# Kernel optimization log

Measured on AMD Instinct MI355X. Metric: run time of the kernel, lower is better.

## Reference

```python
import jax, jax.numpy as jnp
import numpy as np

# dims forced by module structure (see shape_source)
DA, DV, DD, NL, L, R0 = 128, 96, 64, 8, 2, 1.0
ATOMS, EDGES, BATCH = 5000, 40000, 1


def radial_encode_8(rvec, r0):
    # reconstruction: 8 Gaussian RBFs on |r|/r0 with centers k/7
    r = jnp.sqrt(jnp.sum(rvec * rvec, axis=-1) + 1e-12)
    u = r / r0
    k = jnp.arange(NL, dtype=u.dtype)
    return jnp.exp(-0.5 * (u[..., None] * 7.0 - k) ** 2)  # (E, 8)


def tens_sigmoid(x):
    # equivariant sigmoid: rescale vector by bounded function of its norm
    n = jnp.sqrt(jnp.sum(x * x, axis=-1, keepdims=True) + 1e-12)
    return x * (2.0 * jax.nn.sigmoid(n) - 1.0) / n


def _forward(src, dst, r_ij, x_a, x_v, x_d,
             P_000, P_110, P_220, P_011, P_101, P_121, P_211, P_111,
             P_022, P_202, P_112, P_222, P_212,
             W_in_a, W_in_v, W_in_d, W_out_a, W_out_v, W_out_d,
             Wd_a, W1_a, b1_a, W2_a, b2_a, W3_a, b3_a,
             Vd_v, V1_v, V2_v, V3_v):
    b, A = x_a.shape[:2]
    # read-in, then fuse L into the batch dim (high-actv layout)
    a = jnp.einsum('oc,bnc->bno', W_in_a, x_a).reshape(b, A, L, DA).transpose(2, 0, 1, 3).reshape(L * b, A, DA)
    v = jnp.einsum('oc,bnci->bnoi', W_in_v, x_v).reshape(b, A, L, DV, 3).transpose(2, 0, 1, 3, 4).reshape(L * b, A, DV, 3)
    d = jnp.einsum('oc,bncij->bnoij', W_in_d, x_d).reshape(b, A, L, DD, 3, 3).transpose(2, 0, 1, 3, 4, 5).reshape(L * b, A, DD, 3, 3)

    rad = radial_encode_8(r_ij, R0)              # (E, 8)
    rh = tens_sigmoid(r_ij * (7.0 / R0))         # (E, 3)
    pa = rad                                      # (E, 8)
    pv = rad[:, :, None] * rh[:, None, :]         # (E, 8, 3)
    pd = rad[:, :, None, None] * rh[:, None, None, :] * rh[:, None, :, None]  # (E, 8, 3, 3)

    # edge gather (dst nodes)
    aj, vj, dj = a[:, dst], v[:, dst], d[:, dst]

    # Ant16: 13 fused equivariant tensor-product contractions
    psi_a = (jnp.einsum('alc,el,bec->bea', P_000, pa, aj)
             + jnp.einsum('alc,eli,beci->bea', P_110, pv, vj)
             + jnp.einsum('alc,elij,becij->bea', P_220, pd, dj))

    def cross1(P, phi, xv):
        t = lambda j, k: jnp.einsum('vlc,el,bec->bev', P, phi[:, :, j], xv[:, :, :, k])
        return jnp.stack([t(1, 2) - t(2, 1), t(2, 0) - t(0, 2), t(0, 1) - t(1, 0)], axis=-1)

    psi_v = (jnp.einsum('vlc,el,beci->bevi', P_011, pa, vj)
             + jnp.einsum('vlc,eli,bec->bevi', P_101, pv, aj)
             + jnp.einsum('vlc,elj,becij->bevi', P_121, pv, dj)
             + jnp.einsum('vlc,elij,becj->bevi', P_211, pd, vj)
             + cross1(P_111, pv, vj))

    def cross2(P, phid, xv):
        t = lambda k, m: jnp.einsum('dlc,elj,bec->bedj', P, phid[:, :, k, :], xv[:, :, :, m])
        return jnp.stack([t(1, 2) - t(2, 1), t(2, 0) - t(0, 2), t(0, 1) - t(1, 0)], axis=-2)

    psi_d = (jnp.einsum('dlc,el,becij->bedij', P_022, pa, dj)
             + jnp.einsum('dlc,elij,bec->bedij', P_202, pd, aj)
             + jnp.einsum('dlc,eli,becj->bedij', P_112, pv, vj)
             + jnp.einsum('dlc,elik,beckj->bedij', P_222, pd, dj)
             + cross2(P_212, pd, vj))

    # psi_a = psi_a + MLP(psi_a);  MLP(x) = x W_d^T + 3-layer leaky-relu net
    h = jax.nn.leaky_relu(psi_a @ W1_a.T + b1_a, 0.1)
    h = jax.nn.leaky_relu(h @ W2_a.T + b2_a, 0.1)
    psi_a = psi_a + psi_a @ Wd_a.T + h @ W3_a.T + b3_a

    # psi_v = psi_v + VectorMLP(psi_v) (channel linear + tens_sigmoid, equivariant)
    hv = tens_sigmoid(jnp.einsum('oc,beci->beoi', V1_v, psi_v))
    hv = tens_sigmoid(jnp.einsum('oc,beci->beoi', V2_v, hv))
    psi_v = psi_v + jnp.einsum('oc,beci->beoi', Vd_v, psi_v) + jnp.einsum('oc,beci->beoi', V3_v, hv)

    # scatter-reduce messages onto src nodes
    Ba = jnp.zeros_like(a).at[:, src].add(psi_a)
    Bv = jnp.zeros_like(v).at[:, src].add(psi_v)
    Bd = jnp.zeros_like(d).at[:, src].add(psi_d)

    # unfuse L back into the channel dim (low-actv layout), then read out
    Ba = Ba.reshape(L, b, A, DA).transpose(1, 2, 0, 3).reshape(b, A, L * DA)
    Bv = Bv.reshape(L, b, A, DV, 3).transpose(1, 2, 0, 3, 4).reshape(b, A, L * DV, 3)
    Bd = Bd.reshape(L, b, A, DD, 3, 3).transpose(1, 2, 0, 3, 4, 5).reshape(b, A, L * DD, 3, 3)
    return (jnp.einsum('oc,bnc->bno', W_out_a, Ba),
            jnp.einsum('oc,bnci->bnoi', W_out_v, Bv),
            jnp.einsum('oc,bncij->bnoij', W_out_d, Bd))


def setup_inputs() -> dict:
    key = jax.random.key(0)
    ks = iter(jax.random.split(key, 48))
    nrm = lambda *s: jax.random.normal(next(ks), s, dtype=jnp.float32)
    nfac = (NL * max(DA, DV, DD)) ** -0.5
    P = lambda do, di: nrm(do, NL, di) * nfac
    lin = lambda do, di: nrm(do, di) * (di ** -0.5)
    return dict(
        src=jax.random.randint(next(ks), (EDGES,), 0, ATOMS),
        dst=jax.random.randint(next(ks), (EDGES,), 0, ATOMS),
        r_ij=nrm(EDGES, 3),
        x_a=nrm(BATCH, ATOMS, DA), x_v=nrm(BATCH, ATOMS, DV, 3), x_d=nrm(BATCH, ATOMS, DD, 3, 3),
        P_000=P(DA, DA), P_110=P(DA, DV), P_220=P(DA, DD),
        P_011=P(DV, DV), P_101=P(DV, DA), P_121=P(DV, DD), P_211=P(DV, DV), P_111=P(DV, DV),
        P_022=P(DD, DD), P_202=P(DD, DA), P_112=P(DD, DV), P_222=P(DD, DD), P_212=P(DD, DV),
        W_in_a=lin(DA * L, DA), W_in_v=lin(DV * L, DV), W_in_d=lin(DD * L, DD),
        W_out_a=lin(DA, DA * L), W_out_v=lin(DV, DV * L), W_out_d=lin(DD, DD * L),
        Wd_a=lin(DA, DA), W1_a=lin(2 * DA, DA), b1_a=jnp.zeros(2 * DA, jnp.float32),
        W2_a=lin(2 * DA, 2 * DA), b2_a=jnp.zeros(2 * DA, jnp.float32),
        W3_a=lin(DA, 2 * DA), b3_a=jnp.zeros(DA, jnp.float32),
        Vd_v=lin(DV, DV), V1_v=lin(2 * DV, DV), V2_v=lin(2 * DV, 2 * DV), V3_v=lin(DV, 2 * DV),
    )


def reference(src, dst, r_ij, x_a, x_v, x_d,
              P_000, P_110, P_220, P_011, P_101, P_121, P_211, P_111,
              P_022, P_202, P_112, P_222, P_212,
              W_in_a, W_in_v, W_in_d, W_out_a, W_out_v, W_out_d,
              Wd_a, W1_a, b1_a, W2_a, b2_a, W3_a, b3_a,
              Vd_v, V1_v, V2_v, V3_v):
    return _forward(src, dst, r_ij, x_a, x_v, x_d,
                    P_000, P_110, P_220, P_011, P_101, P_121, P_211, P_111,
                    P_022, P_202, P_112, P_222, P_212,
                    W_in_a, W_in_v, W_in_d, W_out_a, W_out_v, W_out_d,
                    Wd_a, W1_a, b1_a, W2_a, b2_a, W3_a, b3_a,
                    Vd_v, V1_v, V2_v, V3_v)
```

## Files before the change

### kernel.cpp

```cpp
#include <hip/hip_runtime.h>
#include <hip/hip_bf16.h>

#define NA 5000
#define NE 40000

static const int POFF[13] = {0, 131072, 229376, 294912, 368640, 466944, 516096,
                             589824, 663552, 696320, 761856, 811008, 843776};
#define A_OFF    892928
#define V_OFF    2172928
#define D_OFF    5052928
#define PHI_OFF  10812928
#define PSIA_OFF 11292928
#define PSIV_OFF 16412928
#define PSID_OFF 27932928
#define INT_OFF  50972928
#define ICNT  0
#define ICUR  5000
#define SCNT  10000
#define SCUR  15000
#define IOFF  20000
#define SOFF  25008
#define IEIDX 30016
#define ISLOT 70016
#define SPERM 110016

#define OUT_V 640000
#define OUT_D 2080000

#define WT1 0
#define WT2 32768
#define WT3 98304
#define WTD 131072
#define VT1 147456
#define VT2 165888
#define VT3 202752
#define VTD 221184

#define OFF_000 POFF[0]
#define OFF_110 POFF[1]
#define OFF_220 POFF[2]
#define OFF_011 POFF[3]
#define OFF_101 POFF[4]
#define OFF_121 POFF[5]
#define OFF_211 POFF[6]
#define OFF_111 POFF[7]
#define OFF_022 POFF[8]
#define OFF_202 POFF[9]
#define OFF_112 POFF[10]
#define OFF_222 POFF[11]
#define OFF_212 POFF[12]

__device__ __forceinline__ float dot4f(float4 a, float4 b) {
  return a.x*b.x + a.y*b.y + a.z*b.z + a.w*b.w;
}
__device__ __forceinline__ float lrelu(float x) { return x > 0.f ? x : 0.1f*x; }
__device__ __forceinline__ float bf2f(unsigned short u) {
  union { unsigned int i; float f; } x; x.i = ((unsigned int)u) << 16; return x.f;
}
__device__ __forceinline__ unsigned short f2bf(float f) {
  union { unsigned int i; float f; } x; x.f = f;
  unsigned int r = x.i + 0x7FFFu + ((x.i >> 16) & 1u);
  return (unsigned short)(r >> 16);
}

__global__ __launch_bounds__(256) void transposeP_kernel(
    const float* __restrict__ src, float* __restrict__ dst, int O, int C)
{
  int idx = blockIdx.x * 256 + threadIdx.x;
  if (idx >= O * C) return;
  int o = idx / C, c = idx % C;
#pragma unroll
  for (int k = 0; k < 8; ++k)
    dst[((size_t)c * O + o) * 8 + k] = src[((size_t)o * 8 + k) * C + c];
}

__global__ __launch_bounds__(256) void transW_kernel(
    const float* __restrict__ src, float* __restrict__ dst, int R, int C)
{
  int idx = blockIdx.x * 256 + threadIdx.x;
  if (idx >= R * C) return;
  int r = idx / C, c = idx % C;
  dst[(size_t)c * R + r] = src[idx];
}

__global__ __launch_bounds__(256) void hist_kernel(const int* __restrict__ key, int* __restrict__ cnt) {
  int e = blockIdx.x * 256 + threadIdx.x;
  if (e < NE) atomicAdd(&cnt[key[e]], 1);
}

__global__ __launch_bounds__(256) void scan_kernel(const int* __restrict__ cnt, int* __restrict__ off) {
  __shared__ int part[256];
  const int t = threadIdx.x;
  int loc[20]; int s = 0;
#pragma unroll
  for (int i = 0; i < 20; ++i) {
    int idx = t * 20 + i;
    int v = (idx < NA) ? cnt[idx] : 0;
    loc[i] = v; s += v;
  }
  part[t] = s; __syncthreads();
  for (int ofs = 1; ofs < 256; ofs <<= 1) {
    int v = (t >= ofs) ? part[t - ofs] : 0;
    __syncthreads();
    part[t] += v;
    __syncthreads();
  }
  int run = part[t] - s;
#pragma unroll
  for (int i = 0; i < 20; ++i) {
    int idx = t * 20 + i;
    if (idx < NA) off[idx] = run;
    run += loc[i];
  }
  if (t == 255) off[NA] = run;
}

__global__ __launch_bounds__(256) void sort_scatter_kernel(
    const int* __restrict__ dst, const int* __restrict__ off,
    int* __restrict__ cur, int* __restrict__ eidx, int* __restrict__ islot)
{
  int e = blockIdx.x * 256 + threadIdx.x;
  if (e >= NE) return;
  int d = dst[e];
  int pos = off[d] + atomicAdd(&cur[d], 1);
  eidx[pos] = e;
  islot[e] = pos;
}

__global__ __launch_bounds__(256) void ssort_kernel(
    const int* __restrict__ src, const int* __restrict__ islot,
    const int* __restrict__ soff, int* __restrict__ scur, int* __restrict__ sperm)
{
  int e = blockIdx.x * 256 + threadIdx.x;
  if (e >= NE) return;
  int s = src[e];
  int pos = soff[s] + atomicAdd(&scur[s], 1);
  sperm[pos] = islot[e];
}

__global__ __launch_bounds__(256) void phi_kernel(
    const int* __restrict__ eidx, const float* __restrict__ r_ij, float* __restrict__ phi)
{
  int p = blockIdx.x * 256 + threadIdx.x;
  if (p >= NE) return;
  int e = eidx[p];
  const float rx = r_ij[e*3+0], ry = r_ij[e*3+1], rz = r_ij[e*3+2];
  const float r2 = rx*rx + ry*ry + rz*rz;
  const float r = sqrtf(r2 + 1e-12f);
#pragma unroll
  for (int k = 0; k < 8; ++k) {
    const float z = 7.f*r - (float)k;
    phi[(size_t)p*12 + k] = expf(-0.5f*z*z);
  }
  const float nn = sqrtf(49.f*r2 + 1e-12f);
  const float sc = (2.f / (1.f + expf(-nn)) - 1.f) / nn;
  phi[(size_t)p*12 + 8]  = 7.f*rx*sc;
  phi[(size_t)p*12 + 9]  = 7.f*ry*sc;
  phi[(size_t)p*12 + 10] = 7.f*rz*sc;
  phi[(size_t)p*12 + 11] = 0.f;
}

__global__ __launch_bounds__(256) void proj_in_kernel(
    const float* __restrict__ x_a, const float* __restrict__ x_v, const float* __restrict__ x_d,
    const float* __restrict__ Wa, const float* __restrict__ Wv, const float* __restrict__ Wd,
    float* __restrict__ a_ws, float* __restrict__ v_ws, float* __restrict__ d_ws)
{
  __shared__ float xs[992];
  const int n = blockIdx.x, t = threadIdx.x;
  for (int q = t; q < 128; q += 256) xs[q]       = x_a[(size_t)n*128 + q];
  for (int q = t; q < 288; q += 256) xs[128 + q] = x_v[(size_t)n*288 + q];
  for (int q = t; q < 576; q += 256) xs[416 + q] = x_d[(size_t)n*576 + q];
  __syncthreads();
  {
    const float* W = &Wa[(size_t)t * 128];
    float acc = 0.f;
    for (int c = 0; c < 128; c += 4) acc += dot4f(*(const float4*)&W[c], *(const float4*)&xs[c]);
    int l = t >> 7, o = t & 127;
    a_ws[((size_t)l*NA + n)*128 + o] = acc;
  }
  if (t < 192) {
    const float* W = &Wv[(size_t)t * 96];
    float a0 = 0.f, a1 = 0.f, a2 = 0.f;
    for (int c = 0; c < 96; ++c) {
      float w = W[c]; const float* x = &xs[128 + c*3];
      a0 = fmaf(w, x[0], a0); a1 = fmaf(w, x[1], a1); a2 = fmaf(w, x[2], a2);
    }
    int l = t / 96, o = t % 96;
    float* dstp = &v_ws[(((size_t)l*NA + n)*96 + o)*3];
    dstp[0] = a0; dstp[1] = a1; dstp[2] = a2;
  }
  if (t < 128) {
    const float* W = &Wd[(size_t)t * 64];
    float acc[9] = {0,0,0,0,0,0,0,0,0};
    for (int c = 0; c < 64; ++c) {
      float w = W[c]; const float* x = &xs[416 + c*9];
#pragma unroll
      for (int j = 0; j < 9; ++j) acc[j] = fmaf(w, x[j], acc[j]);
    }
    int l = t >> 6, o = t & 63;
    float* dstp = &d_ws[(((size_t)l*NA + n)*64 + o)*9];
#pragma unroll
    for (int j = 0; j < 9; ++j) dstp[j] = acc[j];
  }
}

template<int O, int C, int NMU>
__device__ __forceinline__ void zcompute(const float* __restrict__ Pt,
    const float* __restrict__ xl, int o, float z[8][NMU])
{
#pragma unroll
  for (int k = 0; k < 8; ++k)
#pragma unroll
    for (int m = 0; m < NMU; ++m) z[k][m] = 0.f;
  const float* p = Pt + o * 8;
#pragma unroll 2
  for (int c = 0; c < C; ++c, p += O*8) {
    const float4 pa = *(const float4*)p;
    const float4 pb = *(const float4*)(p + 4);
#pragma unroll
    for (int m = 0; m < NMU; ++m) {
      const float xv = xl[c * NMU + m];
      z[0][m] = fmaf(pa.x, xv, z[0][m]);
      z[1][m] = fmaf(pa.y, xv, z[1][m]);
      z[2][m] = fmaf(pa.z, xv, z[2][m]);
      z[3][m] = fmaf(pa.w, xv, z[3][m]);
      z[4][m] = fmaf(pb.x, xv, z[4][m]);
      z[5][m] = fmaf(pb.y, xv, z[5][m]);
      z[6][m] = fmaf(pb.z, xv, z[6][m]);
      z[7][m] = fmaf(pb.w, xv, z[7][m]);
    }
  }
}

template<int O, int C>
__device__ __forceinline__ void zcompute_k4(const float* __restrict__ Pt,
    const float* __restrict__ xl, int o, int kh, float z[4][9])
{
#pragma unroll
  for (int k = 0; k < 4; ++k)
#pragma unroll
    for (int m = 0; m < 9; ++m) z[k][m] = 0.f;
  const float* p = Pt + o * 8 + kh * 4;
#pragma unroll 2
  for (int c = 0; c < C; ++c, p += O*8) {
    const float4 pa = *(const float4*)p;
#pragma unroll
    for (int m = 0; m < 9; ++m) {
      const float xv = xl[c*9 + m];
      z[0][m] = fmaf(pa.x, xv, z[0][m]);
      z[1][m] = fmaf(pa.y, xv, z[1][m]);
      z[2][m] = fmaf(pa.z, xv, z[2][m]);
      z[3][m] = fmaf(pa.w, xv, z[3][m]);
    }
  }
}

template<int NMU>
__device__ __forceinline__ float kdot(const float z[8][NMU], int m, const float* rr) {
  float s = z[0][m] * rr[0];
#pragma unroll
  for (int k = 1; k < 8; ++k) s = fmaf(z[k][m], rr[k], s);
  return s;
}
__device__ __forceinline__ float kdot_k4(const float z[4][9], int m, const float* rr) {
  float s = z[0][m] * rr[0];
#pragma unroll
  for (int k = 1; k < 4; ++k) s = fmaf(z[k][m], rr[k], s);
  return s;
}

#define F1_XA 0
#define F1_XV 256
#define F1_XD 832
#define F1_TOT 1984

template<int NT>
__device__ __forceinline__ void load_features1(float* sm, int t, int n,
    const float* __restrict__ a_ws, const float* __restrict__ v_ws, const float* __restrict__ d_ws)
{
  for (int q = t; q < 256; q += NT)
    sm[F1_XA + q] = a_ws[((size_t)(q>>7)*NA + n)*128 + (q & 127)];
  for (int q = t; q < 576; q += NT)
    sm[F1_XV + q] = v_ws[((size_t)(q/288)*NA + n)*288 + (q % 288)];
  for (int q = t; q < 1152; q += NT)
    sm[F1_XD + q] = d_ws[((size_t)(q/576)*NA + n)*576 + (q % 576)];
}

__global__ __launch_bounds__(256, 3) void pass_a_kernel(
    const int* __restrict__ off, const float* __restrict__ phi,
    const float* __restrict__ Pt,
    const float* __restrict__ a_ws, const float* __restrict__ v_ws, const float* __restrict__ d_ws,
    unsigned short* __restrict__ psiA)
{
  __shared__ float sm[F1_TOT + 192 + 4096];
  const int t = threadIdx.x;
  const int n = blockIdx.x;
  const int off0 = off[n], off1 = off[n + 1];
  const int d = off1 - off0;
  if (d == 0) return;
  const int o = t & 127, l = t >> 7;
  load_features1<256>(sm, t, n, a_ws, v_ws, d_ws);
  const float* xa = &sm[F1_XA + l*128];
  const float* xv = &sm[F1_XV + l*288];
  const float* xd = &sm[F1_XD + l*576];
  float* sphi = &sm[F1_TOT];
  float* psis = &sm[F1_TOT + 192];

  const int nw = (d + 15) >> 4;
  for (int w = 0; w < nw; ++w) {
    const int b0 = w * 16;
    __syncthreads();
    if (t < 192) {
      const int s = t / 12, f = t % 12;
      sphi[t] = (b0 + s < d) ? phi[(size_t)(off0 + b0 + s)*12 + f] : 0.f;
    }
    __syncthreads();

    {
      float z[8][1];
      zcompute<128,128,1>(Pt + OFF_000, xa, o, z);
#pragma unroll
      for (int e = 0; e < 16; ++e)
        psis[e*256 + t] = kdot<1>(z, 0, &sphi[e*12]);
    }
    {
      float z[8][3];
      zcompute<128,96,3>(Pt + OFF_110, xv, o, z);
#pragma unroll
      for (int e = 0; e < 16; ++e) {
        const float* ph = &sphi[e*12];
        psis[e*256 + t] += ph[8]*kdot<3>(z,0,ph) + ph[9]*kdot<3>(z,1,ph) + ph[10]*kdot<3>(z,2,ph);
      }
    }
#pragma unroll
    for (int kh = 0; kh < 2; ++kh) {
      float z[4][9];
      zcompute_k4<128,64>(Pt + OFF_220, xd, o, kh, z);
#pragma unroll
      for (int e = 0; e < 16; ++e) {
        const float* ph = &sphi[e*12];
        const float* rr = ph + kh*4;
        float s[9];
#pragma unroll
        for (int m = 0; m < 9; ++m) s[m] = kdot_k4(z, m, rr);
        const float q0 = ph[8], q1 = ph[9], q2 = ph[10];
        psis[e*256 + t] += q0*(q0*s[0] + q1*s[1] + q2*s[2])
                         + q1*(q0*s[3] + q1*s[4] + q2*s[5])
                         + q2*(q0*s[6] + q1*s[7] + q2*s[8]);
      }
    }
#pragma unroll
    for (int e = 0; e < 16; ++e)
      if (b0 + e < d) psiA[(size_t)(off0 + b0 + e)*256 + t] = f2bf(psis[e*256 + t]);
  }
}

__global__ __launch_bounds__(192, 3) void pass_v_kernel(
    const int* __restrict__ off, const float* __restrict__ phi,
    const float* __restrict__ Pt,
    const float* __restrict__ a_ws, const float* __restrict__ v_ws, const float* __restrict__ d_ws,
    unsigned short* __restrict__ psiV)
{
  __shared__ float sm[F1_TOT + 96 + 4608];
  const int t = threadIdx.x;
  const int n = blockIdx.x;
  const int off0 = off[n], off1 = off[n + 1];
  const int d = off1 - off0;
  if (d == 0) return;
  const int o = t % 96, l = t / 96;
  load_features1<192>(sm, t, n, a_ws, v_ws, d_ws);
  const float* xa = &sm[F1_XA + l*128];
  const float* xv = &sm[F1_XV + l*288];
  const float* xd = &sm[F1_XD + l*576];
  float* sphi = &sm[F1_TOT];
  float* psis = &sm[F1_TOT + 96];

  const int nw = (d + 7) >> 3;
  for (int w = 0; w < nw; ++w) {
    const int b0 = w * 8;
    __syncthreads();
    if (t < 96) {
      const int s = t / 12, f = t % 12;
      sphi[t] = (b0 + s < d) ? phi[(size_t)(off0 + b0 + s)*12 + f] : 0.f;
    }
    __syncthreads();

    {
      float z[8][3];
      zcompute<96,96,3>(Pt + OFF_011, xv, o, z);
#pragma unroll
      for (int e = 0; e < 8; ++e) {
        const float* ph = &sphi[e*12];
        float* pb = &psis[e*576 + t];
        pb[0]   = kdot<3>(z,0,ph);
        pb[192] = kdot<3>(z,1,ph);
        pb[384] = kdot<3>(z,2,ph);
      }
    }
    {
      float z[8][1];
      zcompute<96,128,1>(Pt + OFF_101, xa, o, z);
#pragma unroll
      for (int e = 0; e < 8; ++e) {
        const float* ph = &sphi[e*12];
        const float s0 = kdot<1>(z,0,ph);
        float* pb = &psis[e*576 + t];
        pb[0] += ph[8]*s0; pb[192] += ph[9]*s0; pb[384] += ph[10]*s0;
      }
    }
#pragma unroll
    for (int kh = 0; kh < 2; ++kh) {
      float z[4][9];
      zcompute_k4<96,64>(Pt + OFF_121, xd, o, kh, z);
#pragma unroll
      for (int e = 0; e < 8; ++e) {
        const float* ph = &sphi[e*12];
        const float* rr = ph + kh*4;
        float s[9];
#pragma unroll
        for (int m = 0; m < 9; ++m) s[m] = kdot_k4(z, m, rr);
        const float q0 = ph[8], q1 = ph[9], q2 = ph[10];
        float* pb = &psis[e*576 + t];
        pb[0]   += q0*s[0] + q1*s[1] + q2*s[2];
        pb[192] += q0*s[3] + q1*s[4] + q2*s[5];
        pb[384] += q0*s[6] + q1*s[7] + q2*s[8];
      }
    }
    {
      float z[8][3];
      zcompute<96,96,3>(Pt + OFF_211, xv, o, z);
#pragma unroll
      for (int e = 0; e < 8; ++e) {
        const float* ph = &sphi[e*12];
        const float tt = ph[8]*kdot<3>(z,0,ph) + ph[9]*kdot<3>(z,1,ph) + ph[10]*kdot<3>(z,2,ph);
        float* pb = &psis[e*576 + t];
        pb[0] += ph[8]*tt; pb[192] += ph[9]*tt; pb[384] += ph[10]*tt;
      }
    }
    {
      float z[8][3];
      zcompute<96,96,3>(Pt + OFF_111, xv, o, z);
#pragma unroll
      for (int e = 0; e < 8; ++e) {
        const float* ph = &sphi[e*12];
        const float s0 = kdot<3>(z,0,ph), s1 = kdot<3>(z,1,ph), s2 = kdot<3>(z,2,ph);
        const float q0 = ph[8], q1 = ph[9], q2 = ph[10];
        float* pb = &psis[e*576 + t];
        pb[0]   += q1*s2 - q2*s1;
        pb[192] += q2*s0 - q0*s2;
        pb[384] += q0*s1 - q1*s0;
      }
    }
#pragma unroll
    for (int e = 0; e < 8; ++e) {
      if (b0 + e < d) {
        const size_t b = (size_t)(off0 + b0 + e)*576 + l*288 + o*3;
        const float* pb = &psis[e*576 + t];
        psiV[b+0] = f2bf(pb[0]); psiV[b+1] = f2bf(pb[192]); psiV[b+2] = f2bf(pb[384]);
      }
    }
  }
}

__global__ __launch_bounds__(128, 2) void pass_d_kernel(
    const int* __restrict__ off, const float* __restrict__ phi,
    const float* __restrict__ Pt,
    const float* __restrict__ a_ws, const float* __restrict__ v_ws, const float* __restrict__ d_ws,
    unsigned short* __restrict__ psiD)
{
  __shared__ float sm[F1_TOT + 72 + 6912];
  const int t = threadIdx.x;
  const int n = blockIdx.x;
  const int off0 = off[n], off1 = off[n + 1];
  const int d = off1 - off0;
  if (d == 0) return;
  const int o = t & 63, l = t >> 6;
  load_features1<128>(sm, t, n, a_ws, v_ws, d_ws);
  const float* xa = &sm[F1_XA + l*128];
  const float* xv = &sm[F1_XV + l*288];
  const float* xd = &sm[F1_XD + l*576];
  float* sphi = &sm[F1_TOT];
  float* psis = &sm[F1_TOT + 72];

  const int nw = (d + 5) / 6;
  for (int w = 0; w < nw; ++w) {
    const int b0 = w * 6;
    __syncthreads();
    if (t < 72) {
      const int s = t / 12, f = t % 12;
      sphi[t] = (b0 + s < d) ? phi[(size_t)(off0 + b0 + s)*12 + f] : 0.f;
    }
    __syncthreads();

    {
      float z[4][9];
      zcompute_k4<64,64>(Pt + OFF_022, xd, o, 0, z);
#pragma unroll
      for (int e = 0; e < 6; ++e) {
        const float* rr = &sphi[e*12];
        float* pb = &psis[(e*128 + t)*9];
#pragma unroll
        for (int m = 0; m < 9; ++m) pb[m] = kdot_k4(z, m, rr);
      }
    }
    {
      float z[4][9];
      zcompute_k4<64,64>(Pt + OFF_022, xd, o, 1, z);
#pragma unroll
      for (int e = 0; e < 6; ++e) {
        const float* rr = &sphi[e*12] + 4;
        float* pb = &psis[(e*128 + t)*9];
#pragma unroll
        for (int m = 0; m < 9; ++m) pb[m] += kdot_k4(z, m, rr);
      }
    }
    {
      float z[8][1];
      zcompute<64,128,1>(Pt + OFF_202, xa, o, z);
#pragma unroll
      for (int e = 0; e < 6; ++e) {
        const float* ph = &sphi[e*12];
        const float s0 = kdot<1>(z, 0, ph);
        const float q0 = ph[8], q1 = ph[9], q2 = ph[10];
        float* pb = &psis[(e*128 + t)*9];
        pb[0] += q0*q0*s0; pb[1] += q0*q1*s0; pb[2] += q0*q2*s0;
        pb[3] += q1*q0*s0; pb[4] += q1*q1*s0; pb[5] += q1*q2*s0;
        pb[6] += q2*q0*s0; pb[7] += q2*q1*s0; pb[8] += q2*q2*s0;
      }
    }
    {
      float z[8][3];
      zcompute<64,96,3>(Pt + OFF_112, xv, o, z);
#pragma unroll
      for (int e = 0; e < 6; ++e) {
        const float* ph = &sphi[e*12];
        const float s0 = kdot<3>(z,0,ph), s1 = kdot<3>(z,1,ph), s2 = kdot<3>(z,2,ph);
        const float q0 = ph[8], q1 = ph[9], q2 = ph[10];
        float* pb = &psis[(e*128 + t)*9];
        pb[0] += q0*s0; pb[1] += q0*s1; pb[2] += q0*s2;
        pb[3] += q1*s0; pb[4] += q1*s1; pb[5] += q1*s2;
        pb[6] += q2*s0; pb[7] += q2*s1; pb[8] += q2*s2;
      }
    }
#pragma unroll
    for (int kh = 0; kh < 2; ++kh) {
      float z[4][9];
      zcompute_k4<64,64>(Pt + OFF_222, xd, o, kh, z);
#pragma unroll
      for (int e = 0; e < 6; ++e) {
        const float* ph = &sphi[e*12];
        const float* rr = ph + kh*4;
        float s[9];
#pragma unroll
        for (int m = 0; m < 9; ++m) s[m] = kdot_k4(z, m, rr);
        const float q0 = ph[8], q1 = ph[9], q2 = ph[10];
        const float u0 = q0*s[0] + q1*s[3] + q2*s[6];
        const float u1 = q0*s[1] + q1*s[4] + q2*s[7];
        const float u2 = q0*s[2] + q1*s[5] + q2*s[8];
        float* pb = &psis[(e*128 + t)*9];
        pb[0] += q0*u0; pb[1] += q0*u1; pb[2] += q0*u2;
        pb[3] += q1*u0; pb[4] += q1*u1; pb[5] += q1*u2;
        pb[6] += q2*u0; pb[7] += q2*u1; pb[8] += q2*u2;
      }
    }
    {
      float z[8][3];
      zcompute<64,96,3>(Pt + OFF_212, xv, o, z);
#pragma unroll
      for (int e = 0; e < 6; ++e) {
        const float* ph = &sphi[e*12];
        const float s0 = kdot<3>(z,0,ph), s1 = kdot<3>(z,1,ph), s2 = kdot<3>(z,2,ph);
        const float q0 = ph[8], q1 = ph[9], q2 = ph[10];
        const float c0 = q1*s2 - q2*s1;
        const float c1 = q2*s0 - q0*s2;
        const float c2 = q0*s1 - q1*s0;
        float* pb = &psis[(e*128 + t)*9];
        pb[0] += c0*q0; pb[1] += c0*q1; pb[2] += c0*q2;
        pb[3] += c1*q0; pb[4] += c1*q1; pb[5] += c1*q2;
        pb[6] += c2*q0; pb[7] += c2*q1; pb[8] += c2*q2;
      }
    }
#pragma unroll
    for (int e = 0; e < 6; ++e) {
      if (b0 + e < d) {
        const float* pb = &psis[(e*128 + t)*9];
        unsigned short* bp = &psiD[(size_t)(off0 + b0 + e)*1152 + t*9];
#pragma unroll
        for (int j = 0; j < 9; ++j) bp[j] = f2bf(pb[j]);
      }
    }
  }
}

__global__ __launch_bounds__(256, 4) void mlp_a_kernel(
    unsigned short* __restrict__ psiA,
    const float* __restrict__ Wdt,
    const float* __restrict__ W1t, const float* __restrict__ b1,
    const float* __restrict__ W2t, const float* __restrict__ b2,
    const float* __restrict__ W3t, const float* __restrict__ b3)
{
  __shared__ float PA[16*128];
  __shared__ float H1[16*256];
  __shared__ float H2[16*256];
  const int t = threadIdx.x;
  const int cbase = blockIdx.x * 16;

  for (int q = t; q < 2048; q += 256)
    PA[q] = bf2f(psiA[(size_t)cbase*128 + q]);
  __syncthreads();
  {
    const int p0 = (t & 63) * 4, j0 = (t >> 6) * 4;
    float acc[4][4];
#pragma unroll
    for (int r = 0; r < 4; ++r)
#pragma unroll
      for (int j = 0; j < 4; ++j) acc[r][j] = 0.f;
    for (int c = 0; c < 128; c += 4) {
      float4 wv[4];
#pragma unroll
      for (int cc = 0; cc < 4; ++cc) wv[cc] = *(const float4*)&W1t[(size_t)(c+cc)*256 + p0];
#pragma unroll
      for (int j = 0; j < 4; ++j) {
        const float4 x = *(const float4*)&PA[(j0+j)*128 + c];
        acc[0][j] += wv[0].x*x.x + wv[1].x*x.y + wv[2].x*x.z + wv[3].x*x.w;
        acc[1][j] += wv[0].y*x.x + wv[1].y*x.y + wv[2].y*x.z + wv[3].y*x.w;
        acc[2][j] += wv[0].z*x.x + wv[1].z*x.y + wv[2].z*x.z + wv[3].z*x.w;
        acc[3][j] += wv[0].w*x.x + wv[1].w*x.y + wv[2].w*x.z + wv[3].w*x.w;
      }
    }
    const float bb0 = b1[p0], bb1 = b1[p0+1], bb2 = b1[p0+2], bb3 = b1[p0+3];
#pragma unroll
    for (int j = 0; j < 4; ++j) {
      float4 v; v.x = lrelu(acc[0][j]+bb0); v.y = lrelu(acc[1][j]+bb1);
      v.z = lrelu(acc[2][j]+bb2); v.w = lrelu(acc[3][j]+bb3);
      *(float4*)&H1[(j0+j)*256 + p0] = v;
    }
  }
  __syncthreads();
  {
    const int p0 = (t & 63) * 4, j0 = (t >> 6) * 4;
    float acc[4][4];
#pragma unroll
    for (int r = 0; r < 4; ++r)
#pragma unroll
      for (int j = 0; j < 4; ++j) acc[r][j] = 0.f;
    for (int c = 0; c < 256; c += 4) {
      float4 wv[4];
#pragma unroll
      for (int cc = 0; cc < 4; ++cc) wv[cc] = *(const float4*)&W2t[(size_t)(c+cc)*256 + p0];
#pragma unroll
      for (int j = 0; j < 4; ++j) {
        const float4 x = *(const float4*)&H1[(j0+j)*256 + c];
        acc[0][j] += wv[0].x*x.x + wv[1].x*x.y + wv[2].x*x.z + wv[3].x*x.w;
        acc[1][j] += wv[0].y*x.x + wv[1].y*x.y + wv[2].y*x.z + wv[3].y*x.w;
        acc[2][j] += wv[0].z*x.x + wv[1].z*x.y + wv[2].z*x.z + wv[3].z*x.w;
        acc[3][j] += wv[0].w*x.x + wv[1].w*x.y + wv[2].w*x.z + wv[3].w*x.w;
      }
    }
    const float bb0 = b2[p0], bb1 = b2[p0+1], bb2 = b2[p0+2], bb3 = b2[p0+3];
#pragma unroll
    for (int j = 0; j < 4; ++j) {
      float4 v; v.x = lrelu(acc[0][j]+bb0); v.y = lrelu(acc[1][j]+bb1);
      v.z = lrelu(acc[2][j]+bb2); v.w = lrelu(acc[3][j]+bb3);
      *(float4*)&H2[(j0+j)*256 + p0] = v;
    }
  }
  __syncthreads();
  {
    const int p0 = (t & 63) * 2, j0 = (t >> 6) * 4;
    float acc[2][4];
#pragma unroll
    for (int r = 0; r < 2; ++r)
#pragma unroll
      for (int j = 0; j < 4; ++j) acc[r][j] = 0.f;
    for (int c = 0; c < 128; c += 4) {
      float2 wv[4];
#pragma unroll
      for (int cc = 0; cc < 4; ++cc) wv[cc] = *(const float2*)&Wdt[(size_t)(c+cc)*128 + p0];
#pragma unroll
      for (int j = 0; j < 4; ++j) {
        const float4 x = *(const float4*)&PA[(j0+j)*128 + c];
        acc[0][j] += wv[0].x*x.x + wv[1].x*x.y + wv[2].x*x.z + wv[3].x*x.w;
        acc[1][j] += wv[0].y*x.x + wv[1].y*x.y + wv[2].y*x.z + wv[3].y*x.w;
      }
    }
    for (int c = 0; c < 256; c += 4) {
      float2 wv[4];
#pragma unroll
      for (int cc = 0; cc < 4; ++cc) wv[cc] = *(const float2*)&W3t[(size_t)(c+cc)*128 + p0];
#pragma unroll
      for (int j = 0; j < 4; ++j) {
        const float4 x = *(const float4*)&H2[(j0+j)*256 + c];
        acc[0][j] += wv[0].x*x.x + wv[1].x*x.y + wv[2].x*x.z + wv[3].x*x.w;
        acc[1][j] += wv[0].y*x.x + wv[1].y*x.y + wv[2].y*x.z + wv[3].y*x.w;
      }
    }
    const float bb0 = b3[p0], bb1 = b3[p0+1];
#pragma unroll
    for (int j = 0; j < 4; ++j) {
      const float o0 = acc[0][j] + bb0 + PA[(j0+j)*128 + p0];
      const float o1 = acc[1][j] + bb1 + PA[(j0+j)*128 + p0 + 1];
      psiA[(size_t)(cbase + j0 + j)*128 + p0]     = f2bf(o0);
      psiA[(size_t)(cbase + j0 + j)*128 + p0 + 1] = f2bf(o1);
    }
  }
}

__global__ __launch_bounds__(192, 3) void mlp_v_kernel(
    unsigned short* __restrict__ psiV,
    const float* __restrict__ Vdt, const float* __restrict__ V1t,
    const float* __restrict__ V2t, const float* __restrict__ V3t)
{
  __shared__ float PV[8*288];
  __shared__ float HV[8*576];
  __shared__ float HV2[8*576];
  const int t = threadIdx.x;
  const int cbase = blockIdx.x * 8;

  for (int q = t; q < 2304; q += 192) {
    const int j = q / 288, r = q % 288, i = r / 96, o = r % 96;
    PV[j*288 + i*96 + o] = bf2f(psiV[(size_t)(cbase + j)*288 + o*3 + i]);
  }
  __syncthreads();
  {
    const int p0 = (t % 96) * 2, j0 = (t / 96) * 4;
    float acc[2][4][3];
#pragma unroll
    for (int r = 0; r < 2; ++r)
#pragma unroll
      for (int j = 0; j < 4; ++j) { acc[r][j][0]=0.f; acc[r][j][1]=0.f; acc[r][j][2]=0.f; }
    for (int c = 0; c < 96; c += 4) {
      float2 wv[4];
#pragma unroll
      for (int cc = 0; cc < 4; ++cc) wv[cc] = *(const float2*)&V1t[(size_t)(c+cc)*192 + p0];
#pragma unroll
      for (int j = 0; j < 4; ++j)
#pragma unroll
        for (int i = 0; i < 3; ++i) {
          const float4 x = *(const float4*)&PV[(j0+j)*288 + i*96 + c];
          acc[0][j][i] += wv[0].x*x.x + wv[1].x*x.y + wv[2].x*x.z + wv[3].x*x.w;
          acc[1][j][i] += wv[0].y*x.x + wv[1].y*x.y + wv[2].y*x.z + wv[3].y*x.w;
        }
    }
    float scl[2][4];
#pragma unroll
    for (int r = 0; r < 2; ++r)
#pragma unroll
      for (int j = 0; j < 4; ++j) {
        const float nn = sqrtf(acc[r][j][0]*acc[r][j][0] + acc[r][j][1]*acc[r][j][1]
                             + acc[r][j][2]*acc[r][j][2] + 1e-12f);
        scl[r][j] = (2.f / (1.f + expf(-nn)) - 1.f) / nn;
      }
#pragma unroll
    for (int j = 0; j < 4; ++j)
#pragma unroll
      for (int i = 0; i < 3; ++i) {
        float2 v;
        v.x = acc[0][j][i]*scl[0][j]; v.y = acc[1][j][i]*scl[1][j];
        *(float2*)&HV[(j0+j)*576 + i*192 + p0] = v;
      }
  }
  __syncthreads();
  {
    const int p0 = (t % 96) * 2, j0 = (t / 96) * 4;
    float acc[2][4][3];
#pragma unroll
    for (int r = 0; r < 2; ++r)
#pragma unroll
      for (int j = 0; j < 4; ++j) { acc[r][j][0]=0.f; acc[r][j][1]=0.f; acc[r][j][2]=0.f; }
    for (int c = 0; c < 192; c += 4) {
      float2 wv[4];
#pragma unroll
      for (int cc = 0; cc < 4; ++cc) wv[cc] = *(const float2*)&V2t[(size_t)(c+cc)*192 + p0];
#pragma unroll
      for (int j = 0; j < 4; ++j)
#pragma unroll
        for (int i = 0; i < 3; ++i) {
          const float4 x = *(const float4*)&HV[(j0+j)*576 + i*192 + c];
          acc[0][j][i] += wv[0].x*x.x + wv[1].x*x.y + wv[2].x*x.z + wv[3].x*x.w;
          acc[1][j][i] += wv[0].y*x.x + wv[1].y*x.y + wv[2].y*x.z + wv[3].y*x.w;
        }
    }
    float scl[2][4];
#pragma unroll
    for (int r = 0; r < 2; ++r)
#pragma unroll
      for (int j = 0; j < 4; ++j) {
        const float nn = sqrtf(acc[r][j][0]*acc[r][j][0] + acc[r][j][1]*acc[r][j][1]
                             + acc[r][j][2]*acc[r][j][2] + 1e-12f);
        scl[r][j] = (2.f / (1.f + expf(-nn)) - 1.f) / nn;
      }
#pragma unroll
    for (int j = 0; j < 4; ++j)
#pragma unroll
      for (int i = 0; i < 3; ++i) {
        float2 v;
        v.x = acc[0][j][i]*scl[0][j]; v.y = acc[1][j][i]*scl[1][j];
        *(float2*)&HV2[(j0+j)*576 + i*192 + p0] = v;
      }
  }
  __syncthreads();
  {
    const int p0 = t % 96, j0 = (t / 96) * 4;
    float acc[4][3];
#pragma unroll
    for (int j = 0; j < 4; ++j) { acc[j][0]=0.f; acc[j][1]=0.f; acc[j][2]=0.f; }
    for (int c = 0; c < 96; c += 4) {
      float wv[4];
#pragma unroll
      for (int cc = 0; cc < 4; ++cc) wv[cc] = Vdt[(size_t)(c+cc)*96 + p0];
#pragma unroll
      for (int j = 0; j < 4; ++j)
#pragma unroll
        for (int i = 0; i < 3; ++i) {
          const float4 x = *(const float4*)&PV[(j0+j)*288 + i*96 + c];
          acc[j][i] += wv[0]*x.x + wv[1]*x.y + wv[2]*x.z + wv[3]*x.w;
        }
    }
    for (int c = 0; c < 192; c += 4) {
      float wv[4];
#pragma unroll
      for (int cc = 0; cc < 4; ++cc) wv[cc] = V3t[(size_t)(c+cc)*96 + p0];
#pragma unroll
      for (int j = 0; j < 4; ++j)
#pragma unroll
        for (int i = 0; i < 3; ++i) {
          const float4 x = *(const float4*)&HV2[(j0+j)*576 + i*192 + c];
          acc[j][i] += wv[0]*x.x + wv[1]*x.y + wv[2]*x.z + wv[3]*x.w;
        }
    }
#pragma unroll
    for (int j = 0; j < 4; ++j)
#pragma unroll
      for (int i = 0; i < 3; ++i) {
        const float v = acc[j][i] + PV[(j0+j)*288 + i*96 + p0];
        psiV[(size_t)(cbase + j0 + j)*288 + p0*3 + i] = f2bf(v);
      }
  }
}

__global__ __launch_bounds__(256, 2) void gather_out_kernel(
    const int* __restrict__ soff, const int* __restrict__ sperm,
    const unsigned short* __restrict__ psiA, const unsigned short* __restrict__ psiV,
    const unsigned short* __restrict__ psiD,
    const float* __restrict__ Wa, const float* __restrict__ Wv, const float* __restrict__ Wd,
    float* __restrict__ out)
{
  __shared__ float bs[1984];
  const int n = blockIdx.x, t = threadIdx.x;
  const int s0 = soff[n], s1 = soff[n + 1];
  float acc[8];
#pragma unroll
  for (int u = 0; u < 8; ++u) acc[u] = 0.f;
  for (int p2 = s0; p2 < s1; ++p2) {
    const int slot = sperm[p2];
    const unsigned short* ra = psiA + (size_t)slot * 256;
    const unsigned short* rv = psiV + (size_t)slot * 576;
    const unsigned short* rd = psiD + (size_t)slot * 1152;
#pragma unroll
    for (int u = 0; u < 8; ++u) {
      const int v = t + 256 * u;
      if (v < 256)        acc[u] += bf2f(ra[v]);
      else if (v < 832)   acc[u] += bf2f(rv[v - 256]);
      else if (v < 1984)  acc[u] += bf2f(rd[v - 832]);
    }
  }
#pragma unroll
  for (int u = 0; u < 8; ++u) {
    const int v = t + 256 * u;
    if (v < 1984) bs[v] = acc[u];
  }
  __syncthreads();
  if (t < 128) {
    const float* W = &Wa[(size_t)t * 256];
    float a = 0.f;
    for (int c = 0; c < 256; c += 4) a += dot4f(*(const float4*)&W[c], *(const float4*)&bs[c]);
    out[(size_t)n*128 + t] = a;
  }
  if (t < 96) {
    const float* W = &Wv[(size_t)t * 192];
    float a0 = 0.f, a1 = 0.f, a2 = 0.f;
    for (int c = 0; c < 192; ++c) {
      const float w = W[c]; const float* x = &bs[256 + c*3];
      a0 = fmaf(w, x[0], a0); a1 = fmaf(w, x[1], a1); a2 = fmaf(w, x[2], a2);
    }
    float* d = &out[OUT_V + ((size_t)n*96 + t)*3];
    d[0] = a0; d[1] = a1; d[2] = a2;
  }
  if (t < 64) {
    const float* W = &Wd[(size_t)t * 128];
    float a[9] = {0,0,0,0,0,0,0,0,0};
    for (int c = 0; c < 128; ++c) {
      const float w = W[c]; const float* x = &bs[832 + c*9];
#pragma unroll
      for (int j = 0; j < 9; ++j) a[j] = fmaf(w, x[j], a[j]);
    }
    float* d = &out[OUT_D + ((size_t)n*64 + t)*9];
#pragma unroll
    for (int j = 0; j < 9; ++j) d[j] = a[j];
  }
}

extern "C" void kernel_launch(void* const* d_in, const int* in_sizes, int n_in,
                              void* d_out, int out_size, void* d_ws, size_t ws_size,
                              hipStream_t stream) {
  (void)in_sizes; (void)n_in; (void)out_size; (void)ws_size;
  const int*   src  = (const int*)d_in[0];
  const int*   dst  = (const int*)d_in[1];
  const float* r_ij = (const float*)d_in[2];
  const float* x_a  = (const float*)d_in[3];
  const float* x_v  = (const float*)d_in[4];
  const float* x_d  = (const float*)d_in[5];
  const float* P[13];
  for (int i = 0; i < 13; ++i) P[i] = (const float*)d_in[6 + i];
  const float* W_in_a  = (const float*)d_in[19];
  const float* W_in_v  = (const float*)d_in[20];
  const float* W_in_d  = (const float*)d_in[21];
  const float* W_out_a = (const float*)d_in[22];
  const float* W_out_v = (const float*)d_in[23];
  const float* W_out_d = (const float*)d_in[24];
  const float* Wd_a = (const float*)d_in[25];
  const float* W1   = (const float*)d_in[26];
  const float* b1   = (const float*)d_in[27];
  const float* W2   = (const float*)d_in[28];
  const float* b2   = (const float*)d_in[29];
  const float* W3   = (const float*)d_in[30];
  const float* b3   = (const float*)d_in[31];
  const float* Vd   = (const float*)d_in[32];
  const float* V1   = (const float*)d_in[33];
  const float* V2   = (const float*)d_in[34];
  const float* V3   = (const float*)d_in[35];

  float* ws = (float*)d_ws;
  float* Pt = ws;
  int*   ib = (int*)(ws + INT_OFF);
  unsigned short* psiA = (unsigned short*)(ws + PSIA_OFF);
  unsigned short* psiV = (unsigned short*)(ws + PSIV_OFF);
  unsigned short* psiD = (unsigned short*)(ws + PSID_OFF);
  float* ot = (float*)d_out;

  static const int Od[13] = {128,128,128, 96, 96, 96, 96, 96, 64, 64, 64, 64, 64};
  static const int Cd[13] = {128, 96, 64, 96,128, 64, 96, 96, 64,128, 96, 64, 96};
  for (int i = 0; i < 13; ++i) {
    const int total = Od[i] * Cd[i];
    transposeP_kernel<<<(total + 255) / 256, 256, 0, stream>>>(P[i], Pt + POFF[i], Od[i], Cd[i]);
  }
  transW_kernel<<<(256*128+255)/256, 256, 0, stream>>>(W1,   ot + WT1, 256, 128);
  transW_kernel<<<(256*256+255)/256, 256, 0, stream>>>(W2,   ot + WT2, 256, 256);
  transW_kernel<<<(128*256+255)/256, 256, 0, stream>>>(W3,   ot + WT3, 128, 256);
  transW_kernel<<<(128*128+255)/256, 256, 0, stream>>>(Wd_a, ot + WTD, 128, 128);
  transW_kernel<<<(192*96 +255)/256, 256, 0, stream>>>(V1,   ot + VT1, 192,  96);
  transW_kernel<<<(192*192+255)/256, 256, 0, stream>>>(V2,   ot + VT2, 192, 192);
  transW_kernel<<<(96*192 +255)/256, 256, 0, stream>>>(V3,   ot + VT3,  96, 192);
  transW_kernel<<<(96*96  +255)/256, 256, 0, stream>>>(Vd,   ot + VTD,  96,  96);

  hipMemsetAsync(ib, 0, 20000 * sizeof(int), stream);

  const int egrid = (NE + 255) / 256;
  hist_kernel<<<egrid, 256, 0, stream>>>(dst, ib + ICNT);
  scan_kernel<<<1, 256, 0, stream>>>(ib + ICNT, ib + IOFF);
  sort_scatter_kernel<<<egrid, 256, 0, stream>>>(dst, ib + IOFF, ib + ICUR, ib + IEIDX, ib + ISLOT);
  hist_kernel<<<egrid, 256, 0, stream>>>(src, ib + SCNT);
  scan_kernel<<<1, 256, 0, stream>>>(ib + SCNT, ib + SOFF);
  ssort_kernel<<<egrid, 256, 0, stream>>>(src, ib + ISLOT, ib + SOFF, ib + SCUR, ib + SPERM);
  phi_kernel<<<egrid, 256, 0, stream>>>(ib + IEIDX, r_ij, ws + PHI_OFF);

  proj_in_kernel<<<NA, 256, 0, stream>>>(x_a, x_v, x_d, W_in_a, W_in_v, W_in_d,
                                         ws + A_OFF, ws + V_OFF, ws + D_OFF);

  pass_a_kernel<<<NA, 256, 0, stream>>>(ib + IOFF, ws + PHI_OFF, Pt,
                                        ws + A_OFF, ws + V_OFF, ws + D_OFF, psiA);
  pass_v_kernel<<<NA, 192, 0, stream>>>(ib + IOFF, ws + PHI_OFF, Pt,
                                        ws + A_OFF, ws + V_OFF, ws + D_OFF, psiV);
  pass_d_kernel<<<NA, 128, 0, stream>>>(ib + IOFF, ws + PHI_OFF, Pt,
                                        ws + A_OFF, ws + V_OFF, ws + D_OFF, psiD);

  mlp_a_kernel<<<(2*NE)/16, 256, 0, stream>>>(psiA, ot + WTD, ot + WT1, b1,
                                              ot + WT2, b2, ot + WT3, b3);
  mlp_v_kernel<<<(2*NE)/8, 192, 0, stream>>>(psiV, ot + VTD, ot + VT1, ot + VT2, ot + VT3);

  gather_out_kernel<<<NA, 256, 0, stream>>>(ib + SOFF, ib + SPERM,
                                            psiA, psiV, psiD,
                                            W_out_a, W_out_v, W_out_d, (float*)d_out);
}
```

Measured before the change: 3.797 ms.

## Merge small setup kernels and fuse per-type pass and MLP launches

Folds the 13 P-transposes and 8 weight transposes into two launches, merges the two histograms and two scans, and combines src-sorting with phi computation. It also fuses the three per-type pass kernels into one 3*NA-block launch dispatched by block index, and the two MLP kernels into one launch. The aim is to cut launch count and let different work types run concurrently on the GPU. In exchange, every block now uses 256 threads and the largest shared-memory footprint, which may lower occupancy for the v and d paths that previously used 192 and 128 threads.

```diff
diff --git a/kernel.cpp b/kernel.cpp
--- a/kernel.cpp
+++ b/kernel.cpp
@@ -63,32 +63,59 @@
   return (unsigned short)(r >> 16);
 }
 
-__global__ __launch_bounds__(256) void transposeP_kernel(
-    const float* __restrict__ src, float* __restrict__ dst, int O, int C)
-{
+struct P13 { const float* p[13]; };
+struct P8  { const float* p[8]; };
+
+__global__ __launch_bounds__(256) void transP_all_kernel(P13 ps, float* __restrict__ Pt)
+{
+  static const int Od[13] = {128,128,128, 96, 96, 96, 96, 96, 64, 64, 64, 64, 64};
+  static const int Cd[13] = {128, 96, 64, 96,128, 64, 96, 96, 64,128, 96, 64, 96};
+  static const int POF[13] = {0, 131072, 229376, 294912, 368640, 466944, 516096,
+                              589824, 663552, 696320, 761856, 811008, 843776};
+  static const int CUM[14] = {0,16384,28672,36864,46080,58368,64512,73728,
+                              82944,87040,95232,101376,105472,111616};
   int idx = blockIdx.x * 256 + threadIdx.x;
-  if (idx >= O * C) return;
-  int o = idx / C, c = idx % C;
+  if (idx >= 111616) return;
+  int i = 0;
+  while (idx >= CUM[i+1]) ++i;
+  const int r = idx - CUM[i];
+  const int O = Od[i], C = Cd[i];
+  const int o = r / C, c = r % C;
+  const float* src = ps.p[i];
+  float* dst = Pt + POF[i];
 #pragma unroll
   for (int k = 0; k < 8; ++k)
     dst[((size_t)c * O + o) * 8 + k] = src[((size_t)o * 8 + k) * C + c];
 }
 
-__global__ __launch_bounds__(256) void transW_kernel(
-    const float* __restrict__ src, float* __restrict__ dst, int R, int C)
-{
+__global__ __launch_bounds__(256) void transW_all_kernel(P8 ps, float* __restrict__ ot)
+{
+  static const int R[8]   = {256,256,128,128,192,192, 96, 96};
+  static const int C[8]   = {128,256,256,128, 96,192,192, 96};
+  static const int CUM[9] = {0,32768,98304,131072,147456,165888,202752,221184,230400};
   int idx = blockIdx.x * 256 + threadIdx.x;
-  if (idx >= R * C) return;
-  int r = idx / C, c = idx % C;
-  dst[(size_t)c * R + r] = src[idx];
-}
-
-__global__ __launch_bounds__(256) void hist_kernel(const int* __restrict__ key, int* __restrict__ cnt) {
+  if (idx >= 230400) return;
+  int i = 0;
+  while (idx >= CUM[i+1]) ++i;
+  const int r = idx - CUM[i];
+  const int rr = r / C[i], cc = r % C[i];
+  ot[(size_t)CUM[i] + (size_t)cc * R[i] + rr] = ps.p[i][r];
+}
+
+__global__ __launch_bounds__(256) void hist2_kernel(
+    const int* __restrict__ dstk, const int* __restrict__ srck,
+    int* __restrict__ cntd, int* __restrict__ cnts)
+{
   int e = blockIdx.x * 256 + threadIdx.x;
-  if (e < NE) atomicAdd(&cnt[key[e]], 1);
-}
-
-__global__ __launch_bounds__(256) void scan_kernel(const int* __restrict__ cnt, int* __restrict__ off) {
+  if (e < NE) { atomicAdd(&cntd[dstk[e]], 1); atomicAdd(&cnts[srck[e]], 1); }
+}
+
+__global__ __launch_bounds__(256) void scan2_kernel(
+    const int* __restrict__ cnt0, int* __restrict__ off0,
+    const int* __restrict__ cnt1, int* __restrict__ off1)
+{
+  const int* cnt = (blockIdx.x == 0) ? cnt0 : cnt1;
+  int* off       = (blockIdx.x == 0) ? off0 : off1;
   __shared__ int part[256];
   const int t = threadIdx.x;
   int loc[20]; int s = 0;
@@ -127,37 +154,37 @@
   islot[e] = pos;
 }
 
-__global__ __launch_bounds__(256) void ssort_kernel(
+__global__ __launch_bounds__(256) void ssort_phi_kernel(
     const int* __restrict__ src, const int* __restrict__ islot,
-    const int* __restrict__ soff, int* __restrict__ scur, int* __restrict__ sperm)
-{
-  int e = blockIdx.x * 256 + threadIdx.x;
-  if (e >= NE) return;
-  int s = src[e];
-  int pos = soff[s] + atomicAdd(&scur[s], 1);
-  sperm[pos] = islot[e];
-}
-
-__global__ __launch_bounds__(256) void phi_kernel(
+    const int* __restrict__ soff, int* __restrict__ scur, int* __restrict__ sperm,
     const int* __restrict__ eidx, const float* __restrict__ r_ij, float* __restrict__ phi)
 {
-  int p = blockIdx.x * 256 + threadIdx.x;
-  if (p >= NE) return;
-  int e = eidx[p];
-  const float rx = r_ij[e*3+0], ry = r_ij[e*3+1], rz = r_ij[e*3+2];
-  const float r2 = rx*rx + ry*ry + rz*rz;
-  const float r = sqrtf(r2 + 1e-12f);
-#pragma unroll
-  for (int k = 0; k < 8; ++k) {
-    const float z = 7.f*r - (float)k;
-    phi[(size_t)p*12 + k] = expf(-0.5f*z*z);
-  }
-  const float nn = sqrtf(49.f*r2 + 1e-12f);
-  const float sc = (2.f / (1.f + expf(-nn)) - 1.f) / nn;
-  phi[(size_t)p*12 + 8]  = 7.f*rx*sc;
-  phi[(size_t)p*12 + 9]  = 7.f*ry*sc;
-  phi[(size_t)p*12 + 10] = 7.f*rz*sc;
-  phi[(size_t)p*12 + 11] = 0.f;
+  const int B = (NE + 255) / 256;
+  if ((int)blockIdx.x < B) {
+    int e = blockIdx.x * 256 + threadIdx.x;
+    if (e >= NE) return;
+    int s = src[e];
+    int pos = soff[s] + atomicAdd(&scur[s], 1);
+    sperm[pos] = islot[e];
+  } else {
+    int p = (blockIdx.x - B) * 256 + threadIdx.x;
+    if (p >= NE) return;
+    int e = eidx[p];
+    const float rx = r_ij[e*3+0], ry = r_ij[e*3+1], rz = r_ij[e*3+2];
+    const float r2 = rx*rx + ry*ry + rz*rz;
+    const float r = sqrtf(r2 + 1e-12f);
+#pragma unroll
+    for (int k = 0; k < 8; ++k) {
+      const float z = 7.f*r - (float)k;
+      phi[(size_t)p*12 + k] = expf(-0.5f*z*z);
+    }
+    const float nn = sqrtf(49.f*r2 + 1e-12f);
+    const float sc = (2.f / (1.f + expf(-nn)) - 1.f) / nn;
+    phi[(size_t)p*12 + 8]  = 7.f*rx*sc;
+    phi[(size_t)p*12 + 9]  = 7.f*ry*sc;
+    phi[(size_t)p*12 + 10] = 7.f*rz*sc;
+    phi[(size_t)p*12 + 11] = 0.f;
+  }
 }
 
 __global__ __launch_bounds__(256) void proj_in_kernel(
@@ -286,556 +313,542 @@
     sm[F1_XD + q] = d_ws[((size_t)(q/576)*NA + n)*576 + (q % 576)];
 }
 
-__global__ __launch_bounds__(256, 3) void pass_a_kernel(
+__global__ __launch_bounds__(256, 3) void pass_fused_kernel(
     const int* __restrict__ off, const float* __restrict__ phi,
     const float* __restrict__ Pt,
     const float* __restrict__ a_ws, const float* __restrict__ v_ws, const float* __restrict__ d_ws,
-    unsigned short* __restrict__ psiA)
-{
-  __shared__ float sm[F1_TOT + 192 + 4096];
+    unsigned short* __restrict__ psiA, unsigned short* __restrict__ psiV,
+    unsigned short* __restrict__ psiD)
+{
+  __shared__ float sm[9040];
+  const int b = blockIdx.x;
+  const int type = b % 3;
+  const int n = b / 3;
   const int t = threadIdx.x;
-  const int n = blockIdx.x;
   const int off0 = off[n], off1 = off[n + 1];
   const int d = off1 - off0;
   if (d == 0) return;
-  const int o = t & 127, l = t >> 7;
+
   load_features1<256>(sm, t, n, a_ws, v_ws, d_ws);
-  const float* xa = &sm[F1_XA + l*128];
-  const float* xv = &sm[F1_XV + l*288];
-  const float* xd = &sm[F1_XD + l*576];
-  float* sphi = &sm[F1_TOT];
-  float* psis = &sm[F1_TOT + 192];
-
-  const int nw = (d + 15) >> 4;
-  for (int w = 0; w < nw; ++w) {
-    const int b0 = w * 16;
-    __syncthreads();
-    if (t < 192) {
-      const int s = t / 12, f = t % 12;
-      sphi[t] = (b0 + s < d) ? phi[(size_t)(off0 + b0 + s)*12 + f] : 0.f;
-    }
-    __syncthreads();
-
-    {
-      float z[8][1];
-      zcompute<128,128,1>(Pt + OFF_000, xa, o, z);
+
+  if (type == 0) {
+    const int o = t & 127, l = t >> 7;
+    const float* xa = &sm[F1_XA + l*128];
+    const float* xv = &sm[F1_XV + l*288];
+    const float* xd = &sm[F1_XD + l*576];
+    float* sphi = &sm[F1_TOT];
+    float* psis = &sm[F1_TOT + 192];
+
+    const int nw = (d + 15) >> 4;
+    for (int w = 0; w < nw; ++w) {
+      const int b0 = w * 16;
+      __syncthreads();
+      if (t < 192) {
+        const int s = t / 12, f = t % 12;
+        sphi[t] = (b0 + s < d) ? phi[(size_t)(off0 + b0 + s)*12 + f] : 0.f;
+      }
+      __syncthreads();
+
+      {
+        float z[8][1];
+        zcompute<128,128,1>(Pt + OFF_000, xa, o, z);
+#pragma unroll
+        for (int e = 0; e < 16; ++e)
+          psis[e*256 + t] = kdot<1>(z, 0, &sphi[e*12]);
+      }
+      {
+        float z[8][3];
+        zcompute<128,96,3>(Pt + OFF_110, xv, o, z);
+#pragma unroll
+        for (int e = 0; e < 16; ++e) {
+          const float* ph = &sphi[e*12];
+          psis[e*256 + t] += ph[8]*kdot<3>(z,0,ph) + ph[9]*kdot<3>(z,1,ph) + ph[10]*kdot<3>(z,2,ph);
+        }
+      }
+#pragma unroll
+      for (int kh = 0; kh < 2; ++kh) {
+        float z[4][9];
+        zcompute_k4<128,64>(Pt + OFF_220, xd, o, kh, z);
+#pragma unroll
+        for (int e = 0; e < 16; ++e) {
+          const float* ph = &sphi[e*12];
+          const float* rr = ph + kh*4;
+          float s[9];
+#pragma unroll
+          for (int m = 0; m < 9; ++m) s[m] = kdot_k4(z, m, rr);
+          const float q0 = ph[8], q1 = ph[9], q2 = ph[10];
+          psis[e*256 + t] += q0*(q0*s[0] + q1*s[1] + q2*s[2])
+                           + q1*(q0*s[3] + q1*s[4] + q2*s[5])
+                           + q2*(q0*s[6] + q1*s[7] + q2*s[8]);
+        }
+      }
 #pragma unroll
       for (int e = 0; e < 16; ++e)
-        psis[e*256 + t] = kdot<1>(z, 0, &sphi[e*12]);
-    }
-    {
-      float z[8][3];
-      zcompute<128,96,3>(Pt + OFF_110, xv, o, z);
-#pragma unroll
-      for (int e = 0; e < 16; ++e) {
-        const float* ph = &sphi[e*12];
-        psis[e*256 + t] += ph[8]*kdot<3>(z,0,ph) + ph[9]*kdot<3>(z,1,ph) + ph[10]*kdot<3>(z,2,ph);
-      }
-    }
-#pragma unroll
-    for (int kh = 0; kh < 2; ++kh) {
-      float z[4][9];
-      zcompute_k4<128,64>(Pt + OFF_220, xd, o, kh, z);
-#pragma unroll
-      for (int e = 0; e < 16; ++e) {
-        const float* ph = &sphi[e*12];
-        const float* rr = ph + kh*4;
-        float s[9];
-#pragma unroll
-        for (int m = 0; m < 9; ++m) s[m] = kdot_k4(z, m, rr);
-        const float q0 = ph[8], q1 = ph[9], q2 = ph[10];
-        psis[e*256 + t] += q0*(q0*s[0] + q1*s[1] + q2*s[2])
-                         + q1*(q0*s[3] + q1*s[4] + q2*s[5])
-                         + q2*(q0*s[6] + q1*s[7] + q2*s[8]);
-      }
-    }
-#pragma unroll
-    for (int e = 0; e < 16; ++e)
-      if (b0 + e < d) psiA[(size_t)(off0 + b0 + e)*256 + t] = f2bf(psis[e*256 + t]);
-  }
-}
-
-__global__ __launch_bounds__(192, 3) void pass_v_kernel(
-    const int* __restrict__ off, const float* __restrict__ phi,
-    const float* __restrict__ Pt,
-    const float* __restrict__ a_ws, const float* __restrict__ v_ws, const float* __restrict__ d_ws,
-    unsigned short* __restrict__ psiV)
-{
-  __shared__ float sm[F1_TOT + 96 + 4608];
-  const int t = threadIdx.x;
-  const int n = blockIdx.x;
-  const int off0 = off[n], off1 = off[n + 1];
-  const int d = off1 - off0;
-  if (d == 0) return;
-  const int o = t % 96, l = t / 96;
-  load_features1<192>(sm, t, n, a_ws, v_ws, d_ws);
-  const float* xa = &sm[F1_XA + l*128];
-  const float* xv = &sm[F1_XV + l*288];
-  const float* xd = &sm[F1_XD + l*576];
-  float* sphi = &sm[F1_TOT];
-  float* psis = &sm[F1_TOT + 96];
-
-  const int nw = (d + 7) >> 3;
-  for (int w = 0; w < nw; ++w) {
-    const int b0 = w * 8;
-    __syncthreads();
-    if (t < 96) {
-      const int s = t / 12, f = t % 12;
-      sphi[t] = (b0 + s < d) ? phi[(size_t)(off0 + b0 + s)*12 + f] : 0.f;
-    }
-    __syncthreads();
-
-    {
-      float z[8][3];
-      zcompute<96,96,3>(Pt + OFF_011, xv, o, z);
-#pragma unroll
-      for (int e = 0; e < 8; ++e) {
-        const float* ph = &sphi[e*12];
-        float* pb = &psis[e*576 + t];
-        pb[0]   = kdot<3>(z,0,ph);
-        pb[192] = kdot<3>(z,1,ph);
-        pb[384] = kdot<3>(z,2,ph);
-      }
-    }
-    {
-      float z[8][1];
-      zcompute<96,128,1>(Pt + OFF_101, xa, o, z);
-#pragma unroll
-      for (int e = 0; e < 8; ++e) {
-        const float* ph = &sphi[e*12];
-        const float s0 = kdot<1>(z,0,ph);
-        float* pb = &psis[e*576 + t];
-        pb[0] += ph[8]*s0; pb[192] += ph[9]*s0; pb[384] += ph[10]*s0;
-      }
-    }
-#pragma unroll
-    for (int kh = 0; kh < 2; ++kh) {
-      float z[4][9];
-      zcompute_k4<96,64>(Pt + OFF_121, xd, o, kh, z);
-#pragma unroll
-      for (int e = 0; e < 8; ++e) {
-        const float* ph = &sphi[e*12];
-        const float* rr = ph + kh*4;
-        float s[9];
-#pragma unroll
-        for (int m = 0; m < 9; ++m) s[m] = kdot_k4(z, m, rr);
-        const float q0 = ph[8], q1 = ph[9], q2 = ph[10];
-        float* pb = &psis[e*576 + t];
-        pb[0]   += q0*s[0] + q1*s[1] + q2*s[2];
-        pb[192] += q0*s[3] + q1*s[4] + q2*s[5];
-        pb[384] += q0*s[6] + q1*s[7] + q2*s[8];
-      }
-    }
-    {
-      float z[8][3];
-      zcompute<96,96,3>(Pt + OFF_211, xv, o, z);
-#pragma unroll
-      for (int e = 0; e < 8; ++e) {
-        const float* ph = &sphi[e*12];
-        const float tt = ph[8]*kdot<3>(z,0,ph) + ph[9]*kdot<3>(z,1,ph) + ph[10]*kdot<3>(z,2,ph);
-        float* pb = &psis[e*576 + t];
-        pb[0] += ph[8]*tt; pb[192] += ph[9]*tt; pb[384] += ph[10]*tt;
-      }
-    }
-    {
-      float z[8][3];
-      zcompute<96,96,3>(Pt + OFF_111, xv, o, z);
-#pragma unroll
-      for (int e = 0; e < 8; ++e) {
-        const float* ph = &sphi[e*12];
-        const float s0 = kdot<3>(z,0,ph), s1 = kdot<3>(z,1,ph), s2 = kdot<3>(z,2,ph);
-        const float q0 = ph[8], q1 = ph[9], q2 = ph[10];
-        float* pb = &psis[e*576 + t];
-        pb[0]   += q1*s2 - q2*s1;
-        pb[192] += q2*s0 - q0*s2;
-        pb[384] += q0*s1 - q1*s0;
-      }
-    }
-#pragma unroll
-    for (int e = 0; e < 8; ++e) {
-      if (b0 + e < d) {
-        const size_t b = (size_t)(off0 + b0 + e)*576 + l*288 + o*3;
-        const float* pb = &psis[e*576 + t];
-        psiV[b+0] = f2bf(pb[0]); psiV[b+1] = f2bf(pb[192]); psiV[b+2] = f2bf(pb[384]);
-      }
-    }
-  }
-}
-
-__global__ __launch_bounds__(128, 2) void pass_d_kernel(
-    const int* __restrict__ off, const float* __restrict__ phi,
-    const float* __restrict__ Pt,
-    const float* __restrict__ a_ws, const float* __restrict__ v_ws, const float* __restrict__ d_ws,
-    unsigned short* __restrict__ psiD)
-{
-  __shared__ float sm[F1_TOT + 72 + 6912];
-  const int t = threadIdx.x;
-  const int n = blockIdx.x;
-  const int off0 = off[n], off1 = off[n + 1];
-  const int d = off1 - off0;
-  if (d == 0) return;
-  const int o = t & 63, l = t >> 6;
-  load_features1<128>(sm, t, n, a_ws, v_ws, d_ws);
-  const float* xa = &sm[F1_XA + l*128];
-  const float* xv = &sm[F1_XV + l*288];
-  const float* xd = &sm[F1_XD + l*576];
-  float* sphi = &sm[F1_TOT];
-  float* psis = &sm[F1_TOT + 72];
-
-  const int nw = (d + 5) / 6;
-  for (int w = 0; w < nw; ++w) {
-    const int b0 = w * 6;
-    __syncthreads();
-    if (t < 72) {
-      const int s = t / 12, f = t % 12;
-      sphi[t] = (b0 + s < d) ? phi[(size_t)(off0 + b0 + s)*12 + f] : 0.f;
-    }
-    __syncthreads();
-
-    {
-      float z[4][9];
-      zcompute_k4<64,64>(Pt + OFF_022, xd, o, 0, z);
-#pragma unroll
-      for (int e = 0; e < 6; ++e) {
-        const float* rr = &sphi[e*12];
-        float* pb = &psis[(e*128 + t)*9];
-#pragma unroll
-        for (int m = 0; m < 9; ++m) pb[m] = kdot_k4(z, m, rr);
-      }
-    }
-    {
-      float z[4][9];
-      zcompute_k4<64,64>(Pt + OFF_022, xd, o, 1, z);
-#pragma unroll
-      for (int e = 0; e < 6; ++e) {
-        const float* rr = &sphi[e*12] + 4;
-        float* pb = &psis[(e*128 + t)*9];
-#pragma unroll
-        for (int m = 0; m < 9; ++m) pb[m] += kdot_k4(z, m, rr);
-      }
-    }
-    {
-      float z[8][1];
-      zcompute<64,128,1>(Pt + OFF_202, xa, o, z);
-#pragma unroll
-      for (int e = 0; e < 6; ++e) {
-        const float* ph = &sphi[e*12];
-        const float s0 = kdot<1>(z, 0, ph);
-        const float q0 = ph[8], q1 = ph[9], q2 = ph[10];
-        float* pb = &psis[(e*128 + t)*9];
-        pb[0] += q0*q0*s0; pb[1] += q0*q1*s0; pb[2] += q0*q2*s0;
-        pb[3] += q1*q0*s0; pb[4] += q1*q1*s0; pb[5] += q1*q2*s0;
-        pb[6] += q2*q0*s0; pb[7] += q2*q1*s0; pb[8] += q2*q2*s0;
-      }
-    }
-    {
-      float z[8][3];
-      zcompute<64,96,3>(Pt + OFF_112, xv, o, z);
-#pragma unroll
-      for (int e = 0; e < 6; ++e) {
-        const float* ph = &sphi[e*12];
-        const float s0 = kdot<3>(z,0,ph), s1 = kdot<3>(z,1,ph), s2 = kdot<3>(z,2,ph);
-        const float q0 = ph[8], q1 = ph[9], q2 = ph[10];
-        float* pb = &psis[(e*128 + t)*9];
-        pb[0] += q0*s0; pb[1] += q0*s1; pb[2] += q0*s2;
-        pb[3] += q1*s0; pb[4] += q1*s1; pb[5] += q1*s2;
-        pb[6] += q2*s0; pb[7] += q2*s1; pb[8] += q2*s2;
-      }
-    }
-#pragma unroll
-    for (int kh = 0; kh < 2; ++kh) {
-      float z[4][9];
-      zcompute_k4<64,64>(Pt + OFF_222, xd, o, kh, z);
-#pragma unroll
-      for (int e = 0; e < 6; ++e) {
-        const float* ph = &sphi[e*12];
-        const float* rr = ph + kh*4;
-        float s[9];
-#pragma unroll
-        for (int m = 0; m < 9; ++m) s[m] = kdot_k4(z, m, rr);
-        const float q0 = ph[8], q1 = ph[9], q2 = ph[10];
-        const float u0 = q0*s[0] + q1*s[3] + q2*s[6];
-        const float u1 = q0*s[1] + q1*s[4] + q2*s[7];
-        const float u2 = q0*s[2] + q1*s[5] + q2*s[8];
-        float* pb = &psis[(e*128 + t)*9];
-        pb[0] += q0*u0; pb[1] += q0*u1; pb[2] += q0*u2;
-        pb[3] += q1*u0; pb[4] += q1*u1; pb[5] += q1*u2;
-        pb[6] += q2*u0; pb[7] += q2*u1; pb[8] += q2*u2;
-      }
-    }
-    {
-      float z[8][3];
-      zcompute<64,96,3>(Pt + OFF_212, xv, o, z);
-#pragma unroll
-      for (int e = 0; e < 6; ++e) {
-        const float* ph = &sphi[e*12];
-        const float s0 = kdot<3>(z,0,ph), s1 = kdot<3>(z,1,ph), s2 = kdot<3>(z,2,ph);
-        const float q0 = ph[8], q1 = ph[9], q2 = ph[10];
-        const float c0 = q1*s2 - q2*s1;
-        const float c1 = q2*s0 - q0*s2;
-        const float c2 = q0*s1 - q1*s0;
-        float* pb = &psis[(e*128 + t)*9];
-        pb[0] += c0*q0; pb[1] += c0*q1; pb[2] += c0*q2;
-        pb[3] += c1*q0; pb[4] += c1*q1; pb[5] += c1*q2;
-        pb[6] += c2*q0; pb[7] += c2*q1; pb[8] += c2*q2;
-      }
-    }
-#pragma unroll
-    for (int e = 0; e < 6; ++e) {
-      if (b0 + e < d) {
-        const float* pb = &psis[(e*128 + t)*9];
-        unsigned short* bp = &psiD[(size_t)(off0 + b0 + e)*1152 + t*9];
-#pragma unroll
-        for (int j = 0; j < 9; ++j) bp[j] = f2bf(pb[j]);
-      }
-    }
-  }
-}
-
-__global__ __launch_bounds__(256, 4) void mlp_a_kernel(
-    unsigned short* __restrict__ psiA,
+        if (b0 + e < d) psiA[(size_t)(off0 + b0 + e)*256 + t] = f2bf(psis[e*256 + t]);
+    }
+  } else if (type == 1) {
+    const bool act = (t < 192);
+    const int o = t % 96, l = (t / 96) & 1;
+    const float* xa = &sm[F1_XA + l*128];
+    const float* xv = &sm[F1_XV + l*288];
+    const float* xd = &sm[F1_XD + l*576];
+    float* sphi = &sm[F1_TOT];
+    float* psis = &sm[F1_TOT + 144];
+
+    const int nw = (d + 11) / 12;
+    for (int w = 0; w < nw; ++w) {
+      const int b0 = w * 12;
+      __syncthreads();
+      if (t < 144) {
+        const int s = t / 12, f = t % 12;
+        sphi[t] = (b0 + s < d) ? phi[(size_t)(off0 + b0 + s)*12 + f] : 0.f;
+      }
+      __syncthreads();
+
+      if (act) {
+        {
+          float z[8][3];
+          zcompute<96,96,3>(Pt + OFF_011, xv, o, z);
+#pragma unroll
+          for (int e = 0; e < 12; ++e) {
+            const float* ph = &sphi[e*12];
+            float* pb = &psis[e*576 + t];
+            pb[0]   = kdot<3>(z,0,ph);
+            pb[192] = kdot<3>(z,1,ph);
+            pb[384] = kdot<3>(z,2,ph);
+          }
+        }
+        {
+          float z[8][1];
+          zcompute<96,128,1>(Pt + OFF_101, xa, o, z);
+#pragma unroll
+          for (int e = 0; e < 12; ++e) {
+            const float* ph = &sphi[e*12];
+            const float s0 = kdot<1>(z,0,ph);
+            float* pb = &psis[e*576 + t];
+            pb[0] += ph[8]*s0; pb[192] += ph[9]*s0; pb[384] += ph[10]*s0;
+          }
+        }
+#pragma unroll
+        for (int kh = 0; kh < 2; ++kh) {
+          float z[4][9];
+          zcompute_k4<96,64>(Pt + OFF_121, xd, o, kh, z);
+#pragma unroll
+          for (int e = 0; e < 12; ++e) {
+            const float* ph = &sphi[e*12];
+            const float* rr = ph + kh*4;
+            float s[9];
+#pragma unroll
+            for (int m = 0; m < 9; ++m) s[m] = kdot_k4(z, m, rr);
+            const float q0 = ph[8], q1 = ph[9], q2 = ph[10];
+            float* pb = &psis[e*576 + t];
+            pb[0]   += q0*s[0] + q1*s[1] + q2*s[2];
+            pb[192] += q0*s[3] + q1*s[4] + q2*s[5];
+            pb[384] += q0*s[6] + q1*s[7] + q2*s[8];
+          }
+        }
+        {
+          float z[8][3];
+          zcompute<96,96,3>(Pt + OFF_211, xv, o, z);
+#pragma unroll
+          for (int e = 0; e < 12; ++e) {
+            const float* ph = &sphi[e*12];
+            const float tt = ph[8]*kdot<3>(z,0,ph) + ph[9]*kdot<3>(z,1,ph) + ph[10]*kdot<3>(z,2,ph);
+            float* pb = &psis[e*576 + t];
+            pb[0] += ph[8]*tt; pb[192] += ph[9]*tt; pb[384] += ph[10]*tt;
+          }
+        }
+        {
+          float z[8][3];
+          zcompute<96,96,3>(Pt + OFF_111, xv, o, z);
+#pragma unroll
+          for (int e = 0; e < 12; ++e) {
+            const float* ph = &sphi[e*12];
+            const float s0 = kdot<3>(z,0,ph), s1 = kdot<3>(z,1,ph), s2 = kdot<3>(z,2,ph);
+            const float q0 = ph[8], q1 = ph[9], q2 = ph[10];
+            float* pb = &psis[e*576 + t];
+            pb[0]   += q1*s2 - q2*s1;
+            pb[192] += q2*s0 - q0*s2;
+            pb[384] += q0*s1 - q1*s0;
+          }
+        }
+#pragma unroll
+        for (int e = 0; e < 12; ++e) {
+          if (b0 + e < d) {
+            const size_t bb = (size_t)(off0 + b0 + e)*576 + l*288 + o*3;
+            const float* pb = &psis[e*576 + t];
+            psiV[bb+0] = f2bf(pb[0]); psiV[bb+1] = f2bf(pb[192]); psiV[bb+2] = f2bf(pb[384]);
+          }
+        }
+      }
+    }
+  } else {
+    const bool act = (t < 128);
+    const int o = t & 63, l = (t >> 6) & 1;
+    const float* xa = &sm[F1_XA + l*128];
+    const float* xv = &sm[F1_XV + l*288];
+    const float* xd = &sm[F1_XD + l*576];
+    float* sphi = &sm[F1_TOT];
+    float* psis = &sm[F1_TOT + 72];
+
+    const int nw = (d + 5) / 6;
+    for (int w = 0; w < nw; ++w) {
+      const int b0 = w * 6;
+      __syncthreads();
+      if (t < 72) {
+        const int s = t / 12, f = t % 12;
+        sphi[t] = (b0 + s < d) ? phi[(size_t)(off0 + b0 + s)*12 + f] : 0.f;
+      }
+      __syncthreads();
+
+      if (act) {
+        {
+          float z[4][9];
+          zcompute_k4<64,64>(Pt + OFF_022, xd, o, 0, z);
+#pragma unroll
+          for (int e = 0; e < 6; ++e) {
+            const float* rr = &sphi[e*12];
+            float* pb = &psis[(e*128 + t)*9];
+#pragma unroll
+            for (int m = 0; m < 9; ++m) pb[m] = kdot_k4(z, m, rr);
+          }
+        }
+        {
+          float z[4][9];
+          zcompute_k4<64,64>(Pt + OFF_022, xd, o, 1, z);
+#pragma unroll
+          for (int e = 0; e < 6; ++e) {
+            const float* rr = &sphi[e*12] + 4;
+            float* pb = &psis[(e*128 + t)*9];
+#pragma unroll
+            for (int m = 0; m < 9; ++m) pb[m] += kdot_k4(z, m, rr);
+          }
+        }
+        {
+          float z[8][1];
+          zcompute<64,128,1>(Pt + OFF_202, xa, o, z);
+#pragma unroll
+          for (int e = 0; e < 6; ++e) {
+            const float* ph = &sphi[e*12];
+            const float s0 = kdot<1>(z, 0, ph);
+            const float q0 = ph[8], q1 = ph[9], q2 = ph[10];
+            float* pb = &psis[(e*128 + t)*9];
+            pb[0] += q0*q0*s0; pb[1] += q0*q1*s0; pb[2] += q0*q2*s0;
+            pb[3] += q1*q0*s0; pb[4] += q1*q1*s0; pb[5] += q1*q2*s0;
+            pb[6] += q2*q0*s0; pb[7] += q2*q1*s0; pb[8] += q2*q2*s0;
+          }
+        }
+        {
+          float z[8][3];
+          zcompute<64,96,3>(Pt + OFF_112, xv, o, z);
+#pragma unroll
+          for (int e = 0; e < 6; ++e) {
+            const float* ph = &sphi[e*12];
+            const float s0 = kdot<3>(z,0,ph), s1 = kdot<3>(z,1,ph), s2 = kdot<3>(z,2,ph);
+            const float q0 = ph[8], q1 = ph[9], q2 = ph[10];
+            float* pb = &psis[(e*128 + t)*9];
+            pb[0] += q0*s0; pb[1] += q0*s1; pb[2] += q0*s2;
+            pb[3] += q1*s0; pb[4] += q1*s1; pb[5] += q1*s2;
+            pb[6] += q2*s0; pb[7] += q2*s1; pb[8] += q2*s2;
+          }
+        }
+#pragma unroll
+        for (int kh = 0; kh < 2; ++kh) {
+          float z[4][9];
+          zcompute_k4<64,64>(Pt + OFF_222, xd, o, kh, z);
+#pragma unroll
+          for (int e = 0; e < 6; ++e) {
+            const float* ph = &sphi[e*12];
+            const float* rr = ph + kh*4;
+            float s[9];
+#pragma unroll
+            for (int m = 0; m < 9; ++m) s[m] = kdot_k4(z, m, rr);
+            const float q0 = ph[8], q1 = ph[9], q2 = ph[10];
+            const float u0 = q0*s[0] + q1*s[3] + q2*s[6];
+            const float u1 = q0*s[1] + q1*s[4] + q2*s[7];
+            const float u2 = q0*s[2] + q1*s[5] + q2*s[8];
+            float* pb = &psis[(e*128 + t)*9];
+            pb[0] += q0*u0; pb[1] += q0*u1; pb[2] += q0*u2;
+            pb[3] += q1*u0; pb[4] += q1*u1; pb[5] += q1*u2;
+            pb[6] += q2*u0; pb[7] += q2*u1; pb[8] += q2*u2;
+          }
+        }
+        {
+          float z[8][3];
+          zcompute<64,96,3>(Pt + OFF_212, xv, o, z);
+#pragma unroll
+          for (int e = 0; e < 6; ++e) {
+            const float* ph = &sphi[e*12];
+            const float s0 = kdot<3>(z,0,ph), s1 = kdot<3>(z,1,ph), s2 = kdot<3>(z,2,ph);
+            const float q0 = ph[8], q1 = ph[9], q2 = ph[10];
+            const float c0 = q1*s2 - q2*s1;
+            const float c1 = q2*s0 - q0*s2;
+            const float c2 = q0*s1 - q1*s0;
+            float* pb = &psis[(e*128 + t)*9];
+            pb[0] += c0*q0; pb[1] += c0*q1; pb[2] += c0*q2;
+            pb[3] += c1*q0; pb[4] += c1*q1; pb[5] += c1*q2;
+            pb[6] += c2*q0; pb[7] += c2*q1; pb[8] += c2*q2;
+          }
+        }
+#pragma unroll
+        for (int e = 0; e < 6; ++e) {
+          if (b0 + e < d) {
+            const float* pb = &psis[(e*128 + t)*9];
+            unsigned short* bp = &psiD[(size_t)(off0 + b0 + e)*1152 + t*9];
+#pragma unroll
+            for (int j = 0; j < 9; ++j) bp[j] = f2bf(pb[j]);
+          }
+        }
+      }
+    }
+  }
+}
+
+__global__ __launch_bounds__(256, 3) void mlp_fused_kernel(
+    unsigned short* __restrict__ psiA, unsigned short* __restrict__ psiV,
     const float* __restrict__ Wdt,
     const float* __restrict__ W1t, const float* __restrict__ b1,
     const float* __restrict__ W2t, const float* __restrict__ b2,
-    const float* __restrict__ W3t, const float* __restrict__ b3)
-{
-  __shared__ float PA[16*128];
-  __shared__ float H1[16*256];
-  __shared__ float H2[16*256];
-  const int t = threadIdx.x;
-  const int cbase = blockIdx.x * 16;
-
-  for (int q = t; q < 2048; q += 256)
-    PA[q] = bf2f(psiA[(size_t)cbase*128 + q]);
-  __syncthreads();
-  {
-    const int p0 = (t & 63) * 4, j0 = (t >> 6) * 4;
-    float acc[4][4];
-#pragma unroll
-    for (int r = 0; r < 4; ++r)
-#pragma unroll
-      for (int j = 0; j < 4; ++j) acc[r][j] = 0.f;
-    for (int c = 0; c < 128; c += 4) {
-      float4 wv[4];
-#pragma unroll
-      for (int cc = 0; cc < 4; ++cc) wv[cc] = *(const float4*)&W1t[(size_t)(c+cc)*256 + p0];
-#pragma unroll
-      for (int j = 0; j < 4; ++j) {
-        const float4 x = *(const float4*)&PA[(j0+j)*128 + c];
-        acc[0][j] += wv[0].x*x.x + wv[1].x*x.y + wv[2].x*x.z + wv[3].x*x.w;
-        acc[1][j] += wv[0].y*x.x + wv[1].y*x.y + wv[2].y*x.z + wv[3].y*x.w;
-        acc[2][j] += wv[0].z*x.x + wv[1].z*x.y + wv[2].z*x.z + wv[3].z*x.w;
-        acc[3][j] += wv[0].w*x.x + wv[1].w*x.y + wv[2].w*x.z + wv[3].w*x.w;
-      }
-    }
-    const float bb0 = b1[p0], bb1 = b1[p0+1], bb2 = b1[p0+2], bb3 = b1[p0+3];
-#pragma unroll
-    for (int j = 0; j < 4; ++j) {
-      float4 v; v.x = lrelu(acc[0][j]+bb0); v.y = lrelu(acc[1][j]+bb1);
-      v.z = lrelu(acc[2][j]+bb2); v.w = lrelu(acc[3][j]+bb3);
-      *(float4*)&H1[(j0+j)*256 + p0] = v;
-    }
-  }
-  __syncthreads();
-  {
-    const int p0 = (t & 63) * 4, j0 = (t >> 6) * 4;
-    float acc[4][4];
-#pragma unroll
-    for (int r = 0; r < 4; ++r)
-#pragma unroll
-      for (int j = 0; j < 4; ++j) acc[r][j] = 0.f;
-    for (int c = 0; c < 256; c += 4) {
-      float4 wv[4];
-#pragma unroll
-      for (int cc = 0; cc < 4; ++cc) wv[cc] = *(const float4*)&W2t[(size_t)(c+cc)*256 + p0];
-#pragma unroll
-      for (int j = 0; j < 4; ++j) {
-        const float4 x = *(const float4*)&H1[(j0+j)*256 + c];
-        acc[0][j] += wv[0].x*x.x + wv[1].x*x.y + wv[2].x*x.z + wv[3].x*x.w;
-        acc[1][j] += wv[0].y*x.x + wv[1].y*x.y + wv[2].y*x.z + wv[3].y*x.w;
-        acc[2][j] += wv[0].z*x.x + wv[1].z*x.y + wv[2].z*x.z + wv[3].z*x.w;
-        acc[3][j] += wv[0].w*x.x + wv[1].w*x.y + wv[2].w*x.z + wv[3].w*x.w;
-      }
-    }
-    const float bb0 = b2[p0], bb1 = b2[p0+1], bb2 = b2[p0+2], bb3 = b2[p0+3];
-#pragma unroll
-    for (int j = 0; j < 4; ++j) {
-      float4 v; v.x = lrelu(acc[0][j]+bb0); v.y = lrelu(acc[1][j]+bb1);
-      v.z = lrelu(acc[2][j]+bb2); v.w = lrelu(acc[3][j]+bb3);
-      *(float4*)&H2[(j0+j)*256 + p0] = v;
-    }
-  }
-  __syncthreads();
-  {
-    const int p0 = (t & 63) * 2, j0 = (t >> 6) * 4;
-    float acc[2][4];
-#pragma unroll
-    for (int r = 0; r < 2; ++r)
-#pragma unroll
-      for (int j = 0; j < 4; ++j) acc[r][j] = 0.f;
-    for (int c = 0; c < 128; c += 4) {
-      float2 wv[4];
-#pragma unroll
-      for (int cc = 0; cc < 4; ++cc) wv[cc] = *(const float2*)&Wdt[(size_t)(c+cc)*128 + p0];
-#pragma unroll
-      for (int j = 0; j < 4; ++j) {
-        const float4 x = *(const float4*)&PA[(j0+j)*128 + c];
-        acc[0][j] += wv[0].x*x.x + wv[1].x*x.y + wv[2].x*x.z + wv[3].x*x.w;
-        acc[1][j] += wv[0].y*x.x + wv[1].y*x.y + wv[2].y*x.z + wv[3].y*x.w;
-      }
-    }
-    for (int c = 0; c < 256; c += 4) {
-      float2 wv[4];
-#pragma unroll
-      for (int cc = 0; cc < 4; ++cc) wv[cc] = *(const float2*)&W3t[(size_t)(c+cc)*128 + p0];
-#pragma unroll
-      for (int j = 0; j < 4; ++j) {
-        const float4 x = *(const float4*)&H2[(j0+j)*256 + c];
-        acc[0][j] += wv[0].x*x.x + wv[1].x*x.y + wv[2].x*x.z + wv[3].x*x.w;
-        acc[1][j] += wv[0].y*x.x + wv[1].y*x.y + wv[2].y*x.z + wv[3].y*x.w;
-      }
-    }
-    const float bb0 = b3[p0], bb1 = b3[p0+1];
-#pragma unroll
-    for (int j = 0; j < 4; ++j) {
-      const float o0 = acc[0][j] + bb0 + PA[(j0+j)*128 + p0];
-      const float o1 = acc[1][j] + bb1 + PA[(j0+j)*128 + p0 + 1];
-      psiA[(size_t)(cbase + j0 + j)*128 + p0]     = f2bf(o0);
-      psiA[(size_t)(cbase + j0 + j)*128 + p0 + 1] = f2bf(o1);
-    }
-  }
-}
-
-__global__ __launch_bounds__(192, 3) void mlp_v_kernel(
-    unsigned short* __restrict__ psiV,
+    const float* __restrict__ W3t, const float* __restrict__ b3,
     const float* __restrict__ Vdt, const float* __restrict__ V1t,
     const float* __restrict__ V2t, const float* __restrict__ V3t)
 {
-  __shared__ float PV[8*288];
-  __shared__ float HV[8*576];
-  __shared__ float HV2[8*576];
+  __shared__ float sm[11520];
+  const int b = blockIdx.x;
   const int t = threadIdx.x;
-  const int cbase = blockIdx.x * 8;
-
-  for (int q = t; q < 2304; q += 192) {
-    const int j = q / 288, r = q % 288, i = r / 96, o = r % 96;
-    PV[j*288 + i*96 + o] = bf2f(psiV[(size_t)(cbase + j)*288 + o*3 + i]);
-  }
-  __syncthreads();
-  {
-    const int p0 = (t % 96) * 2, j0 = (t / 96) * 4;
-    float acc[2][4][3];
-#pragma unroll
-    for (int r = 0; r < 2; ++r)
-#pragma unroll
-      for (int j = 0; j < 4; ++j) { acc[r][j][0]=0.f; acc[r][j][1]=0.f; acc[r][j][2]=0.f; }
-    for (int c = 0; c < 96; c += 4) {
-      float2 wv[4];
-#pragma unroll
-      for (int cc = 0; cc < 4; ++cc) wv[cc] = *(const float2*)&V1t[(size_t)(c+cc)*192 + p0];
+
+  if (b % 3 == 0) {
+    const int cbase = (b / 3) * 16;
+    float* PA = sm;
+    float* H1 = sm + 2048;
+    float* H2 = sm + 6144;
+
+    for (int q = t; q < 2048; q += 256)
+      PA[q] = bf2f(psiA[(size_t)cbase*128 + q]);
+    __syncthreads();
+    {
+      const int p0 = (t & 63) * 4, j0 = (t >> 6) * 4;
+      float acc[4][4];
+#pragma unroll
+      for (int r = 0; r < 4; ++r)
+#pragma unroll
+        for (int j = 0; j < 4; ++j) acc[r][j] = 0.f;
+      for (int c = 0; c < 128; c += 4) {
+        float4 wv[4];
+#pragma unroll
+        for (int cc = 0; cc < 4; ++cc) wv[cc] = *(const float4*)&W1t[(size_t)(c+cc)*256 + p0];
+#pragma unroll
+        for (int j = 0; j < 4; ++j) {
+          const float4 x = *(const float4*)&PA[(j0+j)*128 + c];
+          acc[0][j] += wv[0].x*x.x + wv[1].x*x.y + wv[2].x*x.z + wv[3].x*x.w;
+          acc[1][j] += wv[0].y*x.x + wv[1].y*x.y + wv[2].y*x.z + wv[3].y*x.w;
+          acc[2][j] += wv[0].z*x.x + wv[1].z*x.y + wv[2].z*x.z + wv[3].z*x.w;
+          acc[3][j] += wv[0].w*x.x + wv[1].w*x.y + wv[2].w*x.z + wv[3].w*x.w;
+        }
+      }
+      const float bb0 = b1[p0], bb1 = b1[p0+1], bb2 = b1[p0+2], bb3 = b1[p0+3];
+#pragma unroll
+      for (int j = 0; j < 4; ++j) {
+        float4 v; v.x = lrelu(acc[0][j]+bb0); v.y = lrelu(acc[1][j]+bb1);
+        v.z = lrelu(acc[2][j]+bb2); v.w = lrelu(acc[3][j]+bb3);
+        *(float4*)&H1[(j0+j)*256 + p0] = v;
+      }
+    }
+    __syncthreads();
+    {
+      const int p0 = (t & 63) * 4, j0 = (t >> 6) * 4;
+      float acc[4][4];
+#pragma unroll
+      for (int r = 0; r < 4; ++r)
+#pragma unroll
+        for (int j = 0; j < 4; ++j) acc[r][j] = 0.f;
+      for (int c = 0; c < 256; c += 4) {
+        float4 wv[4];
+#pragma unroll
+        for (int cc = 0; cc < 4; ++cc) wv[cc] = *(const float4*)&W2t[(size_t)(c+cc)*256 + p0];
+#pragma unroll
+        for (int j = 0; j < 4; ++j) {
+          const float4 x = *(const float4*)&H1[(j0+j)*256 + c];
+          acc[0][j] += wv[0].x*x.x + wv[1].x*x.y + wv[2].x*x.z + wv[3].x*x.w;
+          acc[1][j] += wv[0].y*x.x + wv[1].y*x.y + wv[2].y*x.z + wv[3].y*x.w;
+          acc[2][j] += wv[0].z*x.x + wv[1].z*x.y + wv[2].z*x.z + wv[3].z*x.w;
+          acc[3][j] += wv[0].w*x.x + wv[1].w*x.y + wv[2].w*x.z + wv[3].w*x.w;
+        }
+      }
+      const float bb0 = b2[p0], bb1 = b2[p0+1], bb2 = b2[p0+2], bb3 = b2[p0+3];
+#pragma unroll
+      for (int j = 0; j < 4; ++j) {
+        float4 v; v.x = lrelu(acc[0][j]+bb0); v.y = lrelu(acc[1][j]+bb1);
+        v.z = lrelu(acc[2][j]+bb2); v.w = lrelu(acc[3][j]+bb3);
+        *(float4*)&H2[(j0+j)*256 + p0] = v;
+      }
+    }
+    __syncthreads();
+    {
+      const int p0 = (t & 63) * 2, j0 = (t >> 6) * 4;
+      float acc[2][4];
+#pragma unroll
+      for (int r = 0; r < 2; ++r)
+#pragma unroll
+        for (int j = 0; j < 4; ++j) acc[r][j] = 0.f;
+      for (int c = 0; c < 128; c += 4) {
+        float2 wv[4];
+#pragma unroll
+        for (int cc = 0; cc < 4; ++cc) wv[cc] = *(const float2*)&Wdt[(size_t)(c+cc)*128 + p0];
+#pragma unroll
+        for (int j = 0; j < 4; ++j) {
+          const float4 x = *(const float4*)&PA[(j0+j)*128 + c];
+          acc[0][j] += wv[0].x*x.x + wv[1].x*x.y + wv[2].x*x.z + wv[3].x*x.w;
+          acc[1][j] += wv[0].y*x.x + wv[1].y*x.y + wv[2].y*x.z + wv[3].y*x.w;
+        }
+      }
+      for (int c = 0; c < 256; c += 4) {
+        float2 wv[4];
+#pragma unroll
+        for (int cc = 0; cc < 4; ++cc) wv[cc] = *(const float2*)&W3t[(size_t)(c+cc)*128 + p0];
+#pragma unroll
+        for (int j = 0; j < 4; ++j) {
+          const float4 x = *(const float4*)&H2[(j0+j)*256 + c];
+          acc[0][j] += wv[0].x*x.x + wv[1].x*x.y + wv[2].x*x.z + wv[3].x*x.w;
+          acc[1][j] += wv[0].y*x.x + wv[1].y*x.y + wv[2].y*x.z + wv[3].y*x.w;
+        }
+      }
+      const float bb0 = b3[p0], bb1 = b3[p0+1];
+#pragma unroll
+      for (int j = 0; j < 4; ++j) {
+        const float o0 = acc[0][j] + bb0 + PA[(j0+j)*128 + p0];
+        const float o1 = acc[1][j] + bb1 + PA[(j0+j)*128 + p0 + 1];
+        psiA[(size_t)(cbase + j0 + j)*128 + p0]     = f2bf(o0);
+        psiA[(size_t)(cbase + j0 + j)*128 + p0 + 1] = f2bf(o1);
+      }
+    }
+  } else {
+    const bool act = (t < 192);
+    const int cbase = (b - b/3 - 1) * 8;
+    float* PV  = sm;
+    float* HV  = sm + 2304;
+    float* HV2 = sm + 6912;
+
+    for (int q = t; q < 2304; q += 256) {
+      const int j = q / 288, r = q % 288, i = r / 96, o = r % 96;
+      PV[j*288 + i*96 + o] = bf2f(psiV[(size_t)(cbase + j)*288 + o*3 + i]);
+    }
+    __syncthreads();
+    if (act) {
+      const int p0 = (t % 96) * 2, j0 = (t / 96) * 4;
+      float acc[2][4][3];
+#pragma unroll
+      for (int r = 0; r < 2; ++r)
+#pragma unroll
+        for (int j = 0; j < 4; ++j) { acc[r][j][0]=0.f; acc[r][j][1]=0.f; acc[r][j][2]=0.f; }
+      for (int c = 0; c < 96; c += 4) {
+        float2 wv[4];
+#pragma unroll
+        for (int cc = 0; cc < 4; ++cc) wv[cc] = *(const float2*)&V1t[(size_t)(c+cc)*192 + p0];
+#pragma unroll
+        for (int j = 0; j < 4; ++j)
+#pragma unroll
+          for (int i = 0; i < 3; ++i) {
+            const float4 x = *(const float4*)&PV[(j0+j)*288 + i*96 + c];
+            acc[0][j][i] += wv[0].x*x.x + wv[1].x*x.y + wv[2].x*x.z + wv[3].x*x.w;
+            acc[1][j][i] += wv[0].y*x.x + wv[1].y*x.y + wv[2].y*x.z + wv[3].y*x.w;
+          }
+      }
+      float scl[2][4];
+#pragma unroll
+      for (int r = 0; r < 2; ++r)
+#pragma unroll
+        for (int j = 0; j < 4; ++j) {
+          const float nn = sqrtf(acc[r][j][0]*acc[r][j][0] + acc[r][j][1]*acc[r][j][1]
+                               + acc[r][j][2]*acc[r][j][2] + 1e-12f);
+          scl[r][j] = (2.f / (1.f + expf(-nn)) - 1.f) / nn;
+        }
 #pragma unroll
       for (int j = 0; j < 4; ++j)
 #pragma unroll
         for (int i = 0; i < 3; ++i) {
-          const float4 x = *(const float4*)&PV[(j0+j)*288 + i*96 + c];
-          acc[0][j][i] += wv[0].x*x.x + wv[1].x*x.y + wv[2].x*x.z + wv[3].x*x.w;
-          acc[1][j][i] += wv[0].y*x.x + wv[1].y*x.y + wv[2].y*x.z + wv[3].y*x.w;
-        }
-    }
-    float scl[2][4];
-#pragma unroll
-    for (int r = 0; r < 2; ++r)
-#pragma unroll
-      for (int j = 0; j < 4; ++j) {
-        const float nn = sqrtf(acc[r][j][0]*acc[r][j][0] + acc[r][j][1]*acc[r][j][1]
-                             + acc[r][j][2]*acc[r][j][2] + 1e-12f);
-        scl[r][j] = (2.f / (1.f + expf(-nn)) - 1.f) / nn;
-      }
-#pragma unroll
-    for (int j = 0; j < 4; ++j)
-#pragma unroll
-      for (int i = 0; i < 3; ++i) {
-        float2 v;
-        v.x = acc[0][j][i]*scl[0][j]; v.y = acc[1][j][i]*scl[1][j];
-        *(float2*)&HV[(j0+j)*576 + i*192 + p0] = v;
-      }
-  }
-  __syncthreads();
-  {
-    const int p0 = (t % 96) * 2, j0 = (t / 96) * 4;
-    float acc[2][4][3];
-#pragma unroll
-    for (int r = 0; r < 2; ++r)
-#pragma unroll
-      for (int j = 0; j < 4; ++j) { acc[r][j][0]=0.f; acc[r][j][1]=0.f; acc[r][j][2]=0.f; }
-    for (int c = 0; c < 192; c += 4) {
-      float2 wv[4];
-#pragma unroll
-      for (int cc = 0; cc < 4; ++cc) wv[cc] = *(const float2*)&V2t[(size_t)(c+cc)*192 + p0];
+          float2 v;
+          v.x = acc[0][j][i]*scl[0][j]; v.y = acc[1][j][i]*scl[1][j];
+          *(float2*)&HV[(j0+j)*576 + i*192 + p0] = v;
+        }
+    }
+    __syncthreads();
+    if (act) {
+      const int p0 = (t % 96) * 2, j0 = (t / 96) * 4;
+      float acc[2][4][3];
+#pragma unroll
+      for (int r = 0; r < 2; ++r)
+#pragma unroll
+        for (int j = 0; j < 4; ++j) { acc[r][j][0]=0.f; acc[r][j][1]=0.f; acc[r][j][2]=0.f; }
+      for (int c = 0; c < 192; c += 4) {
+        float2 wv[4];
+#pragma unroll
+        for (int cc = 0; cc < 4; ++cc) wv[cc] = *(const float2*)&V2t[(size_t)(c+cc)*192 + p0];
+#pragma unroll
+        for (int j = 0; j < 4; ++j)
+#pragma unroll
+          for (int i = 0; i < 3; ++i) {
+            const float4 x = *(const float4*)&HV[(j0+j)*576 + i*192 + c];
+            acc[0][j][i] += wv[0].x*x.x + wv[1].x*x.y + wv[2].x*x.z + wv[3].x*x.w;
+            acc[1][j][i] += wv[0].y*x.x + wv[1].y*x.y + wv[2].y*x.z + wv[3].y*x.w;
+          }
+      }
+      float scl[2][4];
+#pragma unroll
+      for (int r = 0; r < 2; ++r)
+#pragma unroll
+        for (int j = 0; j < 4; ++j) {
+          const float nn = sqrtf(acc[r][j][0]*acc[r][j][0] + acc[r][j][1]*acc[r][j][1]
+                               + acc[r][j][2]*acc[r][j][2] + 1e-12f);
+          scl[r][j] = (2.f / (1.f + expf(-nn)) - 1.f) / nn;
+        }
 #pragma unroll
       for (int j = 0; j < 4; ++j)
 #pragma unroll
         for (int i = 0; i < 3; ++i) {
-          const float4 x = *(const float4*)&HV[(j0+j)*576 + i*192 + c];
-          acc[0][j][i] += wv[0].x*x.x + wv[1].x*x.y + wv[2].x*x.z + wv[3].x*x.w;
-          acc[1][j][i] += wv[0].y*x.x + wv[1].y*x.y + wv[2].y*x.z + wv[3].y*x.w;
-        }
-    }
-    float scl[2][4];
-#pragma unroll
-    for (int r = 0; r < 2; ++r)
-#pragma unroll
-      for (int j = 0; j < 4; ++j) {
-        const float nn = sqrtf(acc[r][j][0]*acc[r][j][0] + acc[r][j][1]*acc[r][j][1]
-                             + acc[r][j][2]*acc[r][j][2] + 1e-12f);
-        scl[r][j] = (2.f / (1.f + expf(-nn)) - 1.f) / nn;
-      }
-#pragma unroll
-    for (int j = 0; j < 4; ++j)
-#pragma unroll
-      for (int i = 0; i < 3; ++i) {
-        float2 v;
-        v.x = acc[0][j][i]*scl[0][j]; v.y = acc[1][j][i]*scl[1][j];
-        *(float2*)&HV2[(j0+j)*576 + i*192 + p0] = v;
-      }
-  }
-  __syncthreads();
-  {
-    const int p0 = t % 96, j0 = (t / 96) * 4;
-    float acc[4][3];
-#pragma unroll
-    for (int j = 0; j < 4; ++j) { acc[j][0]=0.f; acc[j][1]=0.f; acc[j][2]=0.f; }
-    for (int c = 0; c < 96; c += 4) {
-      float wv[4];
-#pragma unroll
-      for (int cc = 0; cc < 4; ++cc) wv[cc] = Vdt[(size_t)(c+cc)*96 + p0];
+          float2 v;
+          v.x = acc[0][j][i]*scl[0][j]; v.y = acc[1][j][i]*scl[1][j];
+          *(float2*)&HV2[(j0+j)*576 + i*192 + p0] = v;
+        }
+    }
+    __syncthreads();
+    if (act) {
+      const int p0 = t % 96, j0 = (t / 96) * 4;
+      float acc[4][3];
+#pragma unroll
+      for (int j = 0; j < 4; ++j) { acc[j][0]=0.f; acc[j][1]=0.f; acc[j][2]=0.f; }
+      for (int c = 0; c < 96; c += 4) {
+        float wv[4];
+#pragma unroll
+        for (int cc = 0; cc < 4; ++cc) wv[cc] = Vdt[(size_t)(c+cc)*96 + p0];
+#pragma unroll
+        for (int j = 0; j < 4; ++j)
+#pragma unroll
+          for (int i = 0; i < 3; ++i) {
+            const float4 x = *(const float4*)&PV[(j0+j)*288 + i*96 + c];
+            acc[j][i] += wv[0]*x.x + wv[1]*x.y + wv[2]*x.z + wv[3]*x.w;
+          }
+      }
+      for (int c = 0; c < 192; c += 4) {
+        float wv[4];
+#pragma unroll
+        for (int cc = 0; cc < 4; ++cc) wv[cc] = V3t[(size_t)(c+cc)*96 + p0];
+#pragma unroll
+        for (int j = 0; j < 4; ++j)
+#pragma unroll
+          for (int i = 0; i < 3; ++i) {
+            const float4 x = *(const float4*)&HV2[(j0+j)*576 + i*192 + c];
+            acc[j][i] += wv[0]*x.x + wv[1]*x.y + wv[2]*x.z + wv[3]*x.w;
+          }
+      }
 #pragma unroll
       for (int j = 0; j < 4; ++j)
 #pragma unroll
         for (int i = 0; i < 3; ++i) {
-          const float4 x = *(const float4*)&PV[(j0+j)*288 + i*96 + c];
-          acc[j][i] += wv[0]*x.x + wv[1]*x.y + wv[2]*x.z + wv[3]*x.w;
-        }
-    }
-    for (int c = 0; c < 192; c += 4) {
-      float wv[4];
-#pragma unroll
-      for (int cc = 0; cc < 4; ++cc) wv[cc] = V3t[(size_t)(c+cc)*96 + p0];
-#pragma unroll
-      for (int j = 0; j < 4; ++j)
-#pragma unroll
-        for (int i = 0; i < 3; ++i) {
-          const float4 x = *(const float4*)&HV2[(j0+j)*576 + i*192 + c];
-          acc[j][i] += wv[0]*x.x + wv[1]*x.y + wv[2]*x.z + wv[3]*x.w;
-        }
-    }
-#pragma unroll
-    for (int j = 0; j < 4; ++j)
-#pragma unroll
-      for (int i = 0; i < 3; ++i) {
-        const float v = acc[j][i] + PV[(j0+j)*288 + i*96 + p0];
-        psiV[(size_t)(cbase + j0 + j)*288 + p0*3 + i] = f2bf(v);
-      }
+          const float v = acc[j][i] + PV[(j0+j)*288 + i*96 + p0];
+          psiV[(size_t)(cbase + j0 + j)*288 + p0*3 + i] = f2bf(v);
+        }
+    }
   }
 }
 
@@ -939,45 +952,32 @@
   unsigned short* psiD = (unsigned short*)(ws + PSID_OFF);
   float* ot = (float*)d_out;
 
-  static const int Od[13] = {128,128,128, 96, 96, 96, 96, 96, 64, 64, 64, 64, 64};
-  static const int Cd[13] = {128, 96, 64, 96,128, 64, 96, 96, 64,128, 96, 64, 96};
-  for (int i = 0; i < 13; ++i) {
-    const int total = Od[i] * Cd[i];
-    transposeP_kernel<<<(total + 255) / 256, 256, 0, stream>>>(P[i], Pt + POFF[i], Od[i], Cd[i]);
-  }
-  transW_kernel<<<(256*128+255)/256, 256, 0, stream>>>(W1,   ot + WT1, 256, 128);
-  transW_kernel<<<(256*256+255)/256, 256, 0, stream>>>(W2,   ot + WT2, 256, 256);
-  transW_kernel<<<(128*256+255)/256, 256, 0, stream>>>(W3,   ot + WT3, 128, 256);
-  transW_kernel<<<(128*128+255)/256, 256, 0, stream>>>(Wd_a, ot + WTD, 128, 128);
-  transW_kernel<<<(192*96 +255)/256, 256, 0, stream>>>(V1,   ot + VT1, 192,  96);
-  transW_kernel<<<(192*192+255)/256, 256, 0, stream>>>(V2,   ot + VT2, 192, 192);
-  transW_kernel<<<(96*192 +255)/256, 256, 0, stream>>>(V3,   ot + VT3,  96, 192);
-  transW_kernel<<<(96*96  +255)/256, 256, 0, stream>>>(Vd,   ot + VTD,  96,  96);
+  P13 ps; for (int i = 0; i < 13; ++i) ps.p[i] = P[i];
+  transP_all_kernel<<<(111616 + 255) / 256, 256, 0, stream>>>(ps, Pt);
+  P8 pw;
+  pw.p[0] = W1; pw.p[1] = W2; pw.p[2] = W3; pw.p[3] = Wd_a;
+  pw.p[4] = V1; pw.p[5] = V2; pw.p[6] = V3; pw.p[7] = Vd;
+  transW_all_kernel<<<(230400 + 255) / 256, 256, 0, stream>>>(pw, ot);
 
   hipMemsetAsync(ib, 0, 20000 * sizeof(int), stream);
 
   const int egrid = (NE + 255) / 256;
-  hist_kernel<<<egrid, 256, 0, stream>>>(dst, ib + ICNT);
-  scan_kernel<<<1, 256, 0, stream>>>(ib + ICNT, ib + IOFF);
+  hist2_kernel<<<egrid, 256, 0, stream>>>(dst, src, ib + ICNT, ib + SCNT);
+  scan2_kernel<<<2, 256, 0, stream>>>(ib + ICNT, ib + IOFF, ib + SCNT, ib + SOFF);
   sort_scatter_kernel<<<egrid, 256, 0, stream>>>(dst, ib + IOFF, ib + ICUR, ib + IEIDX, ib + ISLOT);
-  hist_kernel<<<egrid, 256, 0, stream>>>(src, ib + SCNT);
-  scan_kernel<<<1, 256, 0, stream>>>(ib + SCNT, ib + SOFF);
-  ssort_kernel<<<egrid, 256, 0, stream>>>(src, ib + ISLOT, ib + SOFF, ib + SCUR, ib + SPERM);
-  phi_kernel<<<egrid, 256, 0, stream>>>(ib + IEIDX, r_ij, ws + PHI_OFF);
+  ssort_phi_kernel<<<2 * egrid, 256, 0, stream>>>(src, ib + ISLOT, ib + SOFF, ib + SCUR,
+                                                  ib + SPERM, ib + IEIDX, r_ij, ws + PHI_OFF);
 
   proj_in_kernel<<<NA, 256, 0, stream>>>(x_a, x_v, x_d, W_in_a, W_in_v, W_in_d,
                                          ws + A_OFF, ws + V_OFF, ws + D_OFF);
 
-  pass_a_kernel<<<NA, 256, 0, stream>>>(ib + IOFF, ws + PHI_OFF, Pt,
-                                        ws + A_OFF, ws + V_OFF, ws + D_OFF, psiA);
-  pass_v_kernel<<<NA, 192, 0, stream>>>(ib + IOFF, ws + PHI_OFF, Pt,
-                                        ws + A_OFF, ws + V_OFF, ws + D_OFF, psiV);
-  pass_d_kernel<<<NA, 128, 0, stream>>>(ib + IOFF, ws + PHI_OFF, Pt,
-                                        ws + A_OFF, ws + V_OFF, ws + D_OFF, psiD);
-
-  mlp_a_kernel<<<(2*NE)/16, 256, 0, stream>>>(psiA, ot + WTD, ot + WT1, b1,
-                                              ot + WT2, b2, ot + WT3, b3);
-  mlp_v_kernel<<<(2*NE)/8, 192, 0, stream>>>(psiV, ot + VTD, ot + VT1, ot + VT2, ot + VT3);
+  pass_fused_kernel<<<3 * NA, 256, 0, stream>>>(ib + IOFF, ws + PHI_OFF, Pt,
+                                                ws + A_OFF, ws + V_OFF, ws + D_OFF,
+                                                psiA, psiV, psiD);
+
+  mlp_fused_kernel<<<15000, 256, 0, stream>>>(psiA, psiV,
+                                              ot + WTD, ot + WT1, b1, ot + WT2, b2, ot + WT3, b3,
+                                              ot + VTD, ot + VT1, ot + VT2, ot + VT3);
 
   gather_out_kernel<<<NA, 256, 0, stream>>>(ib + SOFF, ib + SPERM,
                                             psiA, psiV, psiD,
```

After: 3.406 ms. 10.3% less time.
